# Kernel tuning notes

Hardware: AMD Instinct MI355X
Metric: run time of the kernel (lower is better)

The kernel has to match this reference:

```python
import jax, jax.numpy as jnp
import numpy as np


def _swiglu(h):
    a, b = jnp.split(h, 2, axis=-1)
    return jax.nn.silu(a) * b


def setup_inputs() -> dict:
    key = jax.random.key(0)
    ks = jax.random.split(key, 12)
    B, T, D = 4, 2048, 1024
    HD = 4096          # dense FFN hidden (swiglu -> fc1 out 2*HD)
    S, K = 1024, 4     # ssm d_state, d_conv
    E, HE = 8, 512     # n_experts, expert hidden (swiglu)
    s = 0.02
    w = lambda k_, shape: jax.random.normal(k_, shape, jnp.float32) * s
    return dict(
        x=jax.random.normal(ks[0], (B, T, D), jnp.float32),
        rW=w(ks[1], (3, D)), rb=jnp.zeros((3,), jnp.float32),
        d1W=w(ks[2], (2 * HD, D)), d1b=jnp.zeros((2 * HD,), jnp.float32),
        d2W=w(ks[3], (D, HD)), d2b=jnp.zeros((D,), jnp.float32),
        sW_in=w(ks[4], (S, D)), sb_in=jnp.zeros((S,), jnp.float32),
        sW_conv=w(ks[5], (S, S, K)), sb_conv=jnp.zeros((S,), jnp.float32),
        sW_out=w(ks[6], (D, S)), sb_out=jnp.zeros((D,), jnp.float32),
        mW=w(ks[7], (E, D)), mb=jnp.zeros((E,), jnp.float32),
        eW1=w(ks[8], (E, 2 * HE, D)), eb1=jnp.zeros((E, 2 * HE), jnp.float32),
        eW2=w(ks[9], (E, D, HE)), eb2=jnp.zeros((E, D), jnp.float32),
        k=2,
    )


def reference(x, rW, rb, d1W, d1b, d2W, d2b,
              sW_in, sb_in, sW_conv, sb_conv, sW_out, sb_out,
              mW, mb, eW1, eb1, eW2, eb2, k):
    # ---- branch router (token-level softmax, temperature=1) ----
    bw = jax.nn.softmax(x @ rW.T + rb, axis=-1)              # [B,T,3]

    # ---- branch 0: dense swiglu FFN ----
    dense = _swiglu(x @ d1W.T + d1b) @ d2W.T + d2b           # [B,T,D]

    # ---- branch 1: SSM layer (causal conv, groups=1, gate=1) ----
    h = (x @ sW_in.T + sb_in).transpose(0, 2, 1)             # [B,S,T]
    Kc = sW_conv.shape[-1]
    conv = jax.lax.conv_general_dilated(
        h, sW_conv, window_strides=(1,), padding=[(Kc - 1, 0)],
        dimension_numbers=('NCH', 'OIH', 'NCH'))
    seq = (conv + sb_conv[None, :, None]).transpose(0, 2, 1)  # [B,T,S]
    ssm = seq @ sW_out.T + sb_out                             # [B,T,D]

    # ---- branch 2: MoE (top-k softmax router, dense-dispatch reference) ----
    E = mW.shape[0]
    logits = x @ mW.T + mb                                    # [B,T,E]
    vals, idx = jax.lax.top_k(logits, k)                      # [B,T,k]
    wk = jax.nn.softmax(vals, axis=-1)
    combine = jnp.sum(jax.nn.one_hot(idx, E, dtype=x.dtype) * wk[..., None], axis=-2)  # [B,T,E]
    h1 = _swiglu(jnp.einsum('btd,efd->btef', x, eW1) + eb1)   # [B,T,E,HE]
    eout = jnp.einsum('bteh,edh->bted', h1, eW2) + eb2        # [B,T,E,D]
    moe = jnp.einsum('bted,bte->btd', eout, combine)          # [B,T,D]

    return bw[..., 0:1] * dense + bw[..., 1:2] * ssm + bw[..., 2:3] * moe
```

## Files before the change

kernel.cpp:

```cpp
#include <hip/hip_runtime.h>
#include <hip/hip_bf16.h>
#include <cstdint>

typedef __bf16 bf16_t;
typedef __bf16 bf16x8 __attribute__((ext_vector_type(8)));
typedef float f32x4 __attribute__((ext_vector_type(4)));

#define DEV_INLINE __device__ __forceinline__

#define NTOK 8192
#define DDIM 1024
#define HDIM 4096
#define SDIM 1024
#define NEXP 8
#define HEXP 512
#define TSEQ 2048
#define MAXTILES 136
#define MAXROWS (MAXTILES * 128)

#define VMCNT(n) asm volatile("s_waitcnt vmcnt(" #n ")" ::: "memory")
#define BARF() asm volatile("s_barrier" ::: "memory")

__global__ __launch_bounds__(256) void k_f32_to_bf16(const float* __restrict__ src,
                                                     bf16_t* __restrict__ dst, int n8) {
  int i = blockIdx.x * 256 + threadIdx.x;
  if (i >= n8) return;
  const float4* s = (const float4*)src + (size_t)i * 2;
  float4 v0 = s[0], v1 = s[1];
  bf16x8 o;
  o[0] = (bf16_t)v0.x; o[1] = (bf16_t)v0.y; o[2] = (bf16_t)v0.z; o[3] = (bf16_t)v0.w;
  o[4] = (bf16_t)v1.x; o[5] = (bf16_t)v1.y; o[6] = (bf16_t)v1.z; o[7] = (bf16_t)v1.w;
  *((bf16x8*)dst + i) = o;
}

__global__ __launch_bounds__(256) void k_convw(const float* __restrict__ src,
                                               bf16_t* __restrict__ dst) {
  int i = blockIdx.x * 256 + threadIdx.x;
  size_t flat = (size_t)i * 8;
  int s = (int)(flat >> 12);
  int col = (int)(flat & 4095);
  int k = col >> 10;
  int si0 = col & 1023;
  const float* sp = src + (size_t)s * 4096 + k;
  bf16x8 o;
#pragma unroll
  for (int j = 0; j < 8; ++j) o[j] = (bf16_t)sp[(size_t)(si0 + j) * 4];
  *(bf16x8*)(dst + flat) = o;
}

__global__ __launch_bounds__(256) void k_zero(int* cnt, int* fill, int* idx,
                                              bf16_t* zpad) {
  int i = blockIdx.x * 256 + threadIdx.x;
  if (i < NEXP) { cnt[i] = 0; fill[i] = 0; }
  if (i < 128) zpad[i] = (bf16_t)0.f;
  if (i < MAXROWS) idx[i] = 0;
}

__global__ __launch_bounds__(1024) void k_count(const int* __restrict__ top2e,
                                                int* __restrict__ cnt) {
  __shared__ int hist[NEXP];
  const int tid = threadIdx.x;
  if (tid < NEXP) hist[tid] = 0;
  __syncthreads();
  int c[NEXP];
#pragma unroll
  for (int e = 0; e < NEXP; ++e) c[e] = 0;
#pragma unroll
  for (int j = 0; j < 2 * NTOK / 1024; ++j) {
    int v = top2e[j * 1024 + tid];
#pragma unroll
    for (int e = 0; e < NEXP; ++e) c[e] += (v == e) ? 1 : 0;
  }
#pragma unroll
  for (int e = 0; e < NEXP; ++e)
    for (int off = 32; off; off >>= 1) c[e] += __shfl_xor(c[e], off);
  if ((tid & 63) == 0) {
#pragma unroll
    for (int e = 0; e < NEXP; ++e) atomicAdd(&hist[e], c[e]);
  }
  __syncthreads();
  if (tid < NEXP) cnt[tid] = hist[tid];
}

__global__ void k_scan(const int* __restrict__ cnt, int* __restrict__ base,
                       int* __restrict__ ntiles, int* __restrict__ tile_e,
                       int* __restrict__ tile_row) {
  if (threadIdx.x == 0 && blockIdx.x == 0) {
    int b = 0, tt = 0;
    for (int e = 0; e < NEXP; ++e) {
      base[e] = b;
      int nt = (cnt[e] + 127) >> 7;
      for (int j = 0; j < nt; ++j) { tile_e[tt] = e; tile_row[tt] = b + j * 128; ++tt; }
      b += nt * 128;
    }
    *ntiles = tt;
  }
}

__global__ __launch_bounds__(256) void k_scatter(const int* __restrict__ top2e,
                                                 const float* __restrict__ top2w,
                                                 const int* __restrict__ base,
                                                 int* __restrict__ fill,
                                                 int* __restrict__ idx,
                                                 int* __restrict__ slotmap) {
  __shared__ int lcnt[NEXP];
  __shared__ int lbase[NEXP];
  const int tid = threadIdx.x;
  const int t = blockIdx.x * 256 + tid;
  if (tid < NEXP) lcnt[tid] = 0;
  __syncthreads();
  const int e0 = top2e[t * 2 + 0], e1 = top2e[t * 2 + 1];
  const int s0 = atomicAdd(&lcnt[e0], 1);
  const int s1 = atomicAdd(&lcnt[e1], 1);
  __syncthreads();
  if (tid < NEXP) lbase[tid] = atomicAdd(&fill[tid], lcnt[tid]);
  __syncthreads();
  const int p0 = base[e0] + lbase[e0] + s0;
  const int p1 = base[e1] + lbase[e1] + s1;
  idx[p0] = t; idx[p1] = t;
  slotmap[t * 2 + 0] = p0;
  slotmap[t * 2 + 1] = p1;
}

__global__ __launch_bounds__(256) void k_router(const float* __restrict__ x,
                                                const float* __restrict__ rW,
                                                const float* __restrict__ rb,
                                                const float* __restrict__ mW,
                                                const float* __restrict__ mb,
                                                float* __restrict__ bw3,
                                                int* __restrict__ top2e,
                                                float* __restrict__ top2w) {
  int wave = threadIdx.x >> 6, lane = threadIdx.x & 63;
  int t = blockIdx.x * 4 + wave;
  const float* xr = x + (size_t)t * DDIM;
  float xv[16];
#pragma unroll
  for (int i = 0; i < 16; i += 4) *(float4*)&xv[i] = *(const float4*)&xr[lane * 16 + i];
  float acc[11];
#pragma unroll
  for (int j = 0; j < 11; ++j) {
    const float* w = (j < 3) ? (rW + j * DDIM) : (mW + (j - 3) * DDIM);
    float s = 0.f;
#pragma unroll
    for (int i = 0; i < 16; i += 4) {
      float4 wv = *(const float4*)&w[lane * 16 + i];
      s += xv[i] * wv.x + xv[i + 1] * wv.y + xv[i + 2] * wv.z + xv[i + 3] * wv.w;
    }
    acc[j] = s;
  }
#pragma unroll
  for (int j = 0; j < 11; ++j)
    for (int off = 32; off; off >>= 1) acc[j] += __shfl_xor(acc[j], off);
  if (lane == 0) {
    float l0 = acc[0] + rb[0], l1 = acc[1] + rb[1], l2 = acc[2] + rb[2];
    float mx = fmaxf(l0, fmaxf(l1, l2));
    float e0 = expf(l0 - mx), e1 = expf(l1 - mx), e2 = expf(l2 - mx);
    float inv = 1.f / (e0 + e1 + e2);
    float w2 = e2 * inv;
    bw3[t * 3 + 0] = e0 * inv; bw3[t * 3 + 1] = e1 * inv; bw3[t * 3 + 2] = w2;
    float lg[8];
#pragma unroll
    for (int e = 0; e < 8; ++e) lg[e] = acc[3 + e] + mb[e];
    int i0 = 0;
#pragma unroll
    for (int e = 1; e < 8; ++e) if (lg[e] > lg[i0]) i0 = e;
    int i1 = -1;
#pragma unroll
    for (int e = 0; e < 8; ++e) {
      if (e == i0) continue;
      if (i1 < 0 || lg[e] > lg[i1]) i1 = e;
    }
    float ee = expf(lg[i1] - lg[i0]);
    float w0 = 1.f / (1.f + ee), w1 = ee / (1.f + ee);
    top2e[t * 2 + 0] = i0; top2e[t * 2 + 1] = i1;
    top2w[t * 2 + 0] = w2 * w0; top2w[t * 2 + 1] = w2 * w1;
  }
}

__global__ __launch_bounds__(256) void k_combine(const bf16_t* __restrict__ eo,
                                                 const int* __restrict__ slotmap,
                                                 const float* __restrict__ top2w,
                                                 float* __restrict__ out) {
  int wave = threadIdx.x >> 6, lane = threadIdx.x & 63;
  int t = blockIdx.x * 4 + wave;
  const int s0 = slotmap[t * 2 + 0], s1 = slotmap[t * 2 + 1];
  const float g0 = top2w[t * 2 + 0], g1 = top2w[t * 2 + 1];
  const bf16x8* r0 = (const bf16x8*)(eo + (size_t)s0 * DDIM);
  const bf16x8* r1 = (const bf16x8*)(eo + (size_t)s1 * DDIM);
  float* orow = out + (size_t)t * DDIM;
#pragma unroll
  for (int i = 0; i < 2; ++i) {
    const int d = lane + i * 64;
    bf16x8 a = r0[d], b = r1[d];
    float vo[8];
    *(float4*)&vo[0] = *(const float4*)&orow[d * 8];
    *(float4*)&vo[4] = *(const float4*)&orow[d * 8 + 4];
#pragma unroll
    for (int j = 0; j < 8; ++j) vo[j] += g0 * (float)a[j] + g1 * (float)b[j];
    *(float4*)&orow[d * 8] = *(float4*)&vo[0];
    *(float4*)&orow[d * 8 + 4] = *(float4*)&vo[4];
  }
}

DEV_INLINE void gload16(const bf16_t* g, bf16_t* l) {
  __builtin_amdgcn_global_load_lds((const __attribute__((address_space(1))) void*)g,
                                   (__attribute__((address_space(3))) void*)l, 16, 0, 0);
}

DEV_INLINE void blockmap(int& bx, int& by) {
  const int nbx = gridDim.x, nby = gridDim.y;
  int id = blockIdx.x + nbx * blockIdx.y;
  const int nwg = nbx * nby;
  if ((nwg & 7) == 0) id = (id & 7) * (nwg >> 3) + (id >> 3);
  bx = id % nbx;
  by = id / nbx;
}

constexpr int EPI_BF16 = 0;
constexpr int EPI_OUT_W = 1;
constexpr int EPI_OUT_A = 2;

template <int EPI>
__global__ __launch_bounds__(256) void k_gemm(
    const bf16_t* __restrict__ A, const bf16_t* __restrict__ B,
    bf16_t* __restrict__ Cb, float* __restrict__ Cf,
    const float* __restrict__ bias, const float* __restrict__ scale, int sstride,
    int N, int K) {
  constexpr int BUF = 16384;
  __shared__ __align__(16) char lds[2 * BUF];

  const int tid = threadIdx.x;
  const int lane = tid & 63;
  const int wave = tid >> 6;
  const int lr = lane & 15;
  const int hi = lane >> 4;

  int bx, by;
  blockmap(bx, by);

  const int bm = by * 128;
  const int bn = bx * 128;
  const int wm = (wave >> 1) * 64;
  const int wn = (wave & 1) * 64;

  const int srow = tid >> 2;
  const int scol = 8 * ((tid & 3) ^ ((tid >> 3) & 3));
  const bf16_t* Asrc = A + (size_t)(bm + srow) * K + scol;
  const bf16_t* Bsrc = B + (size_t)(bn + srow) * K + scol;
  const size_t r64K = (size_t)64 * K;
  const int NT = K >> 5;

  f32x4 acc[4][4];
#pragma unroll
  for (int a = 0; a < 4; ++a)
#pragma unroll
    for (int b = 0; b < 4; ++b)
#pragma unroll
      for (int j = 0; j < 4; ++j) acc[a][b][j] = 0.f;

  auto stage = [&](int t) {
    char* l = lds + (t & 1) * BUF + tid * 16;
    const bf16_t* ga = Asrc + (size_t)t * 32;
    const bf16_t* gb = Bsrc + (size_t)t * 32;
    gload16(ga, (bf16_t*)l);
    gload16(ga + r64K, (bf16_t*)(l + 4096));
    gload16(gb, (bf16_t*)(l + 8192));
    gload16(gb + r64K, (bf16_t*)(l + 12288));
  };
  auto rdA = [&](int buf, int row) -> bf16x8 {
    int off = buf + (row << 6) + ((hi ^ ((row >> 1) & 3)) << 4);
    return *(const bf16x8*)(lds + off);
  };
  auto rdB = [&](int buf, int row) -> bf16x8 {
    int off = buf + 8192 + (row << 6) + ((hi ^ ((row >> 1) & 3)) << 4);
    return *(const bf16x8*)(lds + off);
  };

  stage(0);

  for (int t = 0; t < NT; ++t) {
    VMCNT(0);
    BARF();
    const int buf = (t & 1) * BUF;
    bf16x8 bfr[4], afr[4];
#pragma unroll
    for (int ni = 0; ni < 4; ++ni) bfr[ni] = rdB(buf, wn + ni * 16 + lr);
#pragma unroll
    for (int i = 0; i < 4; ++i) afr[i] = rdA(buf, wm + i * 16 + lr);
    if (t + 1 < NT) stage(t + 1);
    __builtin_amdgcn_s_setprio(1);
#pragma unroll
    for (int i = 0; i < 4; ++i)
#pragma unroll
      for (int ni = 0; ni < 4; ++ni)
        acc[i][ni] = __builtin_amdgcn_mfma_f32_16x16x32_bf16(afr[i], bfr[ni], acc[i][ni], 0, 0, 0);
    __builtin_amdgcn_s_setprio(0);
  }

  float bv[4];
#pragma unroll
  for (int ni = 0; ni < 4; ++ni) bv[ni] = bias[bn + wn + ni * 16 + lr];
#pragma unroll
  for (int mi = 0; mi < 4; ++mi) {
#pragma unroll
    for (int j = 0; j < 4; ++j) {
      const int rowg = bm + wm + mi * 16 + hi * 4 + j;
      float sc = 0.f;
      if constexpr (EPI == EPI_OUT_W || EPI == EPI_OUT_A)
        sc = scale[(size_t)rowg * sstride];
#pragma unroll
      for (int ni = 0; ni < 4; ++ni) {
        const int colg = bn + wn + ni * 16 + lr;
        float v = acc[mi][ni][j] + bv[ni];
        if constexpr (EPI == EPI_BF16) {
          Cb[(size_t)rowg * N + colg] = (bf16_t)v;
        } else if constexpr (EPI == EPI_OUT_W) {
          Cf[(size_t)rowg * N + colg] = sc * v;
        } else {
          Cf[(size_t)rowg * N + colg] += sc * v;
        }
      }
    }
  }
}

__global__ __launch_bounds__(256) void k_gemm_fc1(
    const bf16_t* __restrict__ A, const bf16_t* __restrict__ Ba,
    const bf16_t* __restrict__ Bb, bf16_t* __restrict__ C,
    const float* __restrict__ bias_a, const float* __restrict__ bias_b,
    int N, int K) {
  constexpr int BUF = 16384;
  __shared__ __align__(16) char lds[2 * BUF];

  const int tid = threadIdx.x;
  const int lane = tid & 63;
  const int wave = tid >> 6;
  const int lr = lane & 15;
  const int hi = lane >> 4;

  int bx, by;
  blockmap(bx, by);

  const int bm = by * 128;
  const int bn = bx * 64;
  const int wm = (wave >> 1) * 64;
  const int wn = (wave & 1) * 32;

  const int srow = tid >> 2;
  const int scol = 8 * ((tid & 3) ^ ((tid >> 3) & 3));
  const bf16_t* Asrc = A + (size_t)(bm + srow) * K + scol;
  const bf16_t* Basrc = Ba + (size_t)(bn + srow) * K + scol;
  const bf16_t* Bbsrc = Bb + (size_t)(bn + srow) * K + scol;
  const size_t r64K = (size_t)64 * K;
  const int NT = K >> 5;

  f32x4 aca[4][2], acb[4][2];
#pragma unroll
  for (int a = 0; a < 4; ++a)
#pragma unroll
    for (int b = 0; b < 2; ++b)
#pragma unroll
      for (int j = 0; j < 4; ++j) { aca[a][b][j] = 0.f; acb[a][b][j] = 0.f; }

  auto stage = [&](int t) {
    char* l = lds + (t & 1) * BUF + tid * 16;
    const bf16_t* ga = Asrc + (size_t)t * 32;
    gload16(ga, (bf16_t*)l);
    gload16(ga + r64K, (bf16_t*)(l + 4096));
    gload16(Basrc + (size_t)t * 32, (bf16_t*)(l + 8192));
    gload16(Bbsrc + (size_t)t * 32, (bf16_t*)(l + 12288));
  };
  auto rd = [&](int base, int row) -> bf16x8 {
    int off = base + (row << 6) + ((hi ^ ((row >> 1) & 3)) << 4);
    return *(const bf16x8*)(lds + off);
  };

  stage(0);

  for (int t = 0; t < NT; ++t) {
    VMCNT(0);
    BARF();
    const int buf = (t & 1) * BUF;
    bf16x8 afr[4], bfa[2], bfb[2];
#pragma unroll
    for (int i = 0; i < 4; ++i) afr[i] = rd(buf, wm + i * 16 + lr);
#pragma unroll
    for (int ni = 0; ni < 2; ++ni) bfa[ni] = rd(buf + 8192, wn + ni * 16 + lr);
#pragma unroll
    for (int ni = 0; ni < 2; ++ni) bfb[ni] = rd(buf + 12288, wn + ni * 16 + lr);
    if (t + 1 < NT) stage(t + 1);
    __builtin_amdgcn_s_setprio(1);
#pragma unroll
    for (int i = 0; i < 4; ++i)
#pragma unroll
      for (int ni = 0; ni < 2; ++ni) {
        aca[i][ni] = __builtin_amdgcn_mfma_f32_16x16x32_bf16(afr[i], bfa[ni], aca[i][ni], 0, 0, 0);
        acb[i][ni] = __builtin_amdgcn_mfma_f32_16x16x32_bf16(afr[i], bfb[ni], acb[i][ni], 0, 0, 0);
      }
    __builtin_amdgcn_s_setprio(0);
  }

  float bva[2], bvb[2];
#pragma unroll
  for (int ni = 0; ni < 2; ++ni) {
    bva[ni] = bias_a[bn + wn + ni * 16 + lr];
    bvb[ni] = bias_b[bn + wn + ni * 16 + lr];
  }
#pragma unroll
  for (int mi = 0; mi < 4; ++mi) {
#pragma unroll
    for (int j = 0; j < 4; ++j) {
      const int rowg = bm + wm + mi * 16 + hi * 4 + j;
#pragma unroll
      for (int ni = 0; ni < 2; ++ni) {
        const int colg = bn + wn + ni * 16 + lr;
        float va = aca[mi][ni][j] + bva[ni];
        float vb = acb[mi][ni][j] + bvb[ni];
        float s = va / (1.f + __expf(-va));
        C[(size_t)rowg * N + colg] = (bf16_t)(s * vb);
      }
    }
  }
}

__global__ __launch_bounds__(256) void k_gemm_conv(
    const bf16_t* __restrict__ h, const bf16_t* __restrict__ Bw,
    bf16_t* __restrict__ Cb, const float* __restrict__ bias,
    const bf16_t* __restrict__ zpad) {
  constexpr int N = SDIM;
  constexpr int K = SDIM * 4;
  constexpr int BUF = 16384;
  __shared__ __align__(16) char lds[2 * BUF];

  const int tid = threadIdx.x;
  const int lane = tid & 63;
  const int wave = tid >> 6;
  const int lr = lane & 15;
  const int hi = lane >> 4;

  int bx, by;
  blockmap(bx, by);

  const int bm = by * 128;
  const int bn = bx * 128;
  const int wm = (wave >> 1) * 64;
  const int wn = (wave & 1) * 64;

  const int srow = tid >> 2;
  const int scol = 8 * ((tid & 3) ^ ((tid >> 3) & 3));
  const int row0 = bm + srow;
  const int tt0 = row0 & (TSEQ - 1);
  const bf16_t* Bsrc = Bw + (size_t)(bn + srow) * K + scol;
  const size_t r64K = (size_t)64 * K;
  const int NT = K >> 5;

  f32x4 acc[4][4];
#pragma unroll
  for (int a = 0; a < 4; ++a)
#pragma unroll
    for (int b = 0; b < 4; ++b)
#pragma unroll
      for (int j = 0; j < 4; ++j) acc[a][b][j] = 0.f;

  auto stage = [&](int t) {
    char* l = lds + (t & 1) * BUF + tid * 16;
    const int k = t >> 5;
    const int si = (t & 31) * 32 + scol;
    const bf16_t* ga0 = (tt0 + k >= 3)
        ? h + (size_t)(row0 + k - 3) * SDIM + si : zpad;
    const bf16_t* ga1 = h + (size_t)(row0 + 64 + k - 3) * SDIM + si;
    gload16(ga0, (bf16_t*)l);
    gload16(ga1, (bf16_t*)(l + 4096));
    const bf16_t* gb = Bsrc + (size_t)t * 32;
    gload16(gb, (bf16_t*)(l + 8192));
    gload16(gb + r64K, (bf16_t*)(l + 12288));
  };
  auto rdA = [&](int buf, int row) -> bf16x8 {
    int off = buf + (row << 6) + ((hi ^ ((row >> 1) & 3)) << 4);
    return *(const bf16x8*)(lds + off);
  };
  auto rdB = [&](int buf, int row) -> bf16x8 {
    int off = buf + 8192 + (row << 6) + ((hi ^ ((row >> 1) & 3)) << 4);
    return *(const bf16x8*)(lds + off);
  };

  stage(0);

  for (int t = 0; t < NT; ++t) {
    VMCNT(0);
    BARF();
    const int buf = (t & 1) * BUF;
    bf16x8 bfr[4], afr[4];
#pragma unroll
    for (int ni = 0; ni < 4; ++ni) bfr[ni] = rdB(buf, wn + ni * 16 + lr);
#pragma unroll
    for (int i = 0; i < 4; ++i) afr[i] = rdA(buf, wm + i * 16 + lr);
    if (t + 1 < NT) stage(t + 1);
    __builtin_amdgcn_s_setprio(1);
#pragma unroll
    for (int i = 0; i < 4; ++i)
#pragma unroll
      for (int ni = 0; ni < 4; ++ni)
        acc[i][ni] = __builtin_amdgcn_mfma_f32_16x16x32_bf16(afr[i], bfr[ni], acc[i][ni], 0, 0, 0);
    __builtin_amdgcn_s_setprio(0);
  }

  float bv[4];
#pragma unroll
  for (int ni = 0; ni < 4; ++ni) bv[ni] = bias[bn + wn + ni * 16 + lr];
#pragma unroll
  for (int mi = 0; mi < 4; ++mi) {
#pragma unroll
    for (int j = 0; j < 4; ++j) {
      const int rowg = bm + wm + mi * 16 + hi * 4 + j;
#pragma unroll
      for (int ni = 0; ni < 4; ++ni) {
        const int colg = bn + wn + ni * 16 + lr;
        Cb[(size_t)rowg * N + colg] = (bf16_t)(acc[mi][ni][j] + bv[ni]);
      }
    }
  }
}

__global__ __launch_bounds__(256) void k_moe_fc1(
    const bf16_t* __restrict__ A, const bf16_t* __restrict__ Bw, size_t zB,
    bf16_t* __restrict__ C, const float* __restrict__ bias, int bstride,
    const int* __restrict__ ntiles_p, const int* __restrict__ tile_e,
    const int* __restrict__ tile_row, const int* __restrict__ idx,
    int N, int K) {
  constexpr int BUF = 16384;
  __shared__ __align__(16) char lds[2 * BUF];

  const int tid = threadIdx.x;
  const int lane = tid & 63;
  const int wave = tid >> 6;
  const int lr = lane & 15;
  const int hi = lane >> 4;

  const int nbx = gridDim.x, nby = gridDim.y;
  int id = blockIdx.x + nbx * blockIdx.y;
  const int nwg = nbx * nby;
  if ((nwg & 7) == 0) id = (id & 7) * (nwg >> 3) + (id >> 3);
  const int bx = id % nbx;
  const int by = id / nbx;

  const int ntiles = *ntiles_p;
  if (bx >= ntiles) return;
  const int e = tile_e[bx];
  const int bm = tile_row[bx];
  const int bn = by * 64;
  const int wm = (wave >> 1) * 64;
  const int wn = (wave & 1) * 32;

  const int srow = tid >> 2;
  const int scol = 8 * ((tid & 3) ^ ((tid >> 3) & 3));
  const int atok0 = idx[bm + srow];
  const int atok1 = idx[bm + srow + 64];
  const bf16_t* Asrc0 = A + (size_t)atok0 * K + scol;
  const bf16_t* Asrc1 = A + (size_t)atok1 * K + scol;
  const bf16_t* Basrc = Bw + (size_t)e * zB + (size_t)(bn + srow) * K + scol;
  const bf16_t* Bbsrc = Basrc + (size_t)HEXP * K;
  const int NT = K >> 5;

  f32x4 aca[4][2], acb[4][2];
#pragma unroll
  for (int a = 0; a < 4; ++a)
#pragma unroll
    for (int b = 0; b < 2; ++b)
#pragma unroll
      for (int j = 0; j < 4; ++j) { aca[a][b][j] = 0.f; acb[a][b][j] = 0.f; }

  auto stage = [&](int t) {
    char* l = lds + (t & 1) * BUF + tid * 16;
    gload16(Asrc0 + (size_t)t * 32, (bf16_t*)l);
    gload16(Asrc1 + (size_t)t * 32, (bf16_t*)(l + 4096));
    gload16(Basrc + (size_t)t * 32, (bf16_t*)(l + 8192));
    gload16(Bbsrc + (size_t)t * 32, (bf16_t*)(l + 12288));
  };
  auto rd = [&](int base, int row) -> bf16x8 {
    int off = base + (row << 6) + ((hi ^ ((row >> 1) & 3)) << 4);
    return *(const bf16x8*)(lds + off);
  };

  stage(0);

  for (int t = 0; t < NT; ++t) {
    VMCNT(0);
    BARF();
    const int buf = (t & 1) * BUF;
    bf16x8 afr[4], bfa[2], bfb[2];
#pragma unroll
    for (int i = 0; i < 4; ++i) afr[i] = rd(buf, wm + i * 16 + lr);
#pragma unroll
    for (int ni = 0; ni < 2; ++ni) bfa[ni] = rd(buf + 8192, wn + ni * 16 + lr);
#pragma unroll
    for (int ni = 0; ni < 2; ++ni) bfb[ni] = rd(buf + 12288, wn + ni * 16 + lr);
    if (t + 1 < NT) stage(t + 1);
    __builtin_amdgcn_s_setprio(1);
#pragma unroll
    for (int i = 0; i < 4; ++i)
#pragma unroll
      for (int ni = 0; ni < 2; ++ni) {
        aca[i][ni] = __builtin_amdgcn_mfma_f32_16x16x32_bf16(afr[i], bfa[ni], aca[i][ni], 0, 0, 0);
        acb[i][ni] = __builtin_amdgcn_mfma_f32_16x16x32_bf16(afr[i], bfb[ni], acb[i][ni], 0, 0, 0);
      }
    __builtin_amdgcn_s_setprio(0);
  }

  const float* bpa = bias + (size_t)e * bstride;
  const float* bpb = bpa + HEXP;
  float bva[2], bvb[2];
#pragma unroll
  for (int ni = 0; ni < 2; ++ni) {
    bva[ni] = bpa[bn + wn + ni * 16 + lr];
    bvb[ni] = bpb[bn + wn + ni * 16 + lr];
  }
#pragma unroll
  for (int mi = 0; mi < 4; ++mi) {
#pragma unroll
    for (int j = 0; j < 4; ++j) {
      const int slot = bm + wm + mi * 16 + hi * 4 + j;
#pragma unroll
      for (int ni = 0; ni < 2; ++ni) {
        const int colg = bn + wn + ni * 16 + lr;
        float va = aca[mi][ni][j] + bva[ni];
        float vb = acb[mi][ni][j] + bvb[ni];
        float s = va / (1.f + __expf(-va));
        C[(size_t)slot * N + colg] = (bf16_t)(s * vb);
      }
    }
  }
}

__global__ __launch_bounds__(256) void k_moe_fc2(
    const bf16_t* __restrict__ A, const bf16_t* __restrict__ Bw, size_t zB,
    bf16_t* __restrict__ Cb, const float* __restrict__ bias, int bstride,
    const int* __restrict__ ntiles_p, const int* __restrict__ tile_e,
    const int* __restrict__ tile_row,
    int N, int K) {
  constexpr int BUF = 16384;
  __shared__ __align__(16) char lds[2 * BUF];

  const int tid = threadIdx.x;
  const int lane = tid & 63;
  const int wave = tid >> 6;
  const int lr = lane & 15;
  const int hi = lane >> 4;

  const int nbx = gridDim.x, nby = gridDim.y;
  int id = blockIdx.x + nbx * blockIdx.y;
  const int nwg = nbx * nby;
  if ((nwg & 7) == 0) id = (id & 7) * (nwg >> 3) + (id >> 3);
  const int bx = id % nbx;
  const int by = id / nbx;

  const int ntiles = *ntiles_p;
  if (bx >= ntiles) return;
  const int e = tile_e[bx];
  const int bm = tile_row[bx];
  const int bn = by * 128;
  const int wm = (wave >> 1) * 64;
  const int wn = (wave & 1) * 64;

  const int srow = tid >> 2;
  const int scol = 8 * ((tid & 3) ^ ((tid >> 3) & 3));
  const bf16_t* Asrc = A + (size_t)(bm + srow) * K + scol;
  const bf16_t* Bsrc = Bw + (size_t)e * zB + (size_t)(bn + srow) * K + scol;
  const size_t r64K = (size_t)64 * K;
  const int NT = K >> 5;

  f32x4 acc[4][4];
#pragma unroll
  for (int a = 0; a < 4; ++a)
#pragma unroll
    for (int b = 0; b < 4; ++b)
#pragma unroll
      for (int j = 0; j < 4; ++j) acc[a][b][j] = 0.f;

  auto stage = [&](int t) {
    char* l = lds + (t & 1) * BUF + tid * 16;
    gload16(Asrc + (size_t)t * 32, (bf16_t*)l);
    gload16(Asrc + (size_t)t * 32 + r64K, (bf16_t*)(l + 4096));
    gload16(Bsrc + (size_t)t * 32, (bf16_t*)(l + 8192));
    gload16(Bsrc + (size_t)t * 32 + r64K, (bf16_t*)(l + 12288));
  };
  auto rdA = [&](int buf, int row) -> bf16x8 {
    int off = buf + (row << 6) + ((hi ^ ((row >> 1) & 3)) << 4);
    return *(const bf16x8*)(lds + off);
  };
  auto rdB = [&](int buf, int row) -> bf16x8 {
    int off = buf + 8192 + (row << 6) + ((hi ^ ((row >> 1) & 3)) << 4);
    return *(const bf16x8*)(lds + off);
  };

  stage(0);

  for (int t = 0; t < NT; ++t) {
    VMCNT(0);
    BARF();
    const int buf = (t & 1) * BUF;
    bf16x8 bfr[4], afr[4];
#pragma unroll
    for (int ni = 0; ni < 4; ++ni) bfr[ni] = rdB(buf, wn + ni * 16 + lr);
#pragma unroll
    for (int i = 0; i < 4; ++i) afr[i] = rdA(buf, wm + i * 16 + lr);
    if (t + 1 < NT) stage(t + 1);
    __builtin_amdgcn_s_setprio(1);
#pragma unroll
    for (int i = 0; i < 4; ++i)
#pragma unroll
      for (int ni = 0; ni < 4; ++ni)
        acc[i][ni] = __builtin_amdgcn_mfma_f32_16x16x32_bf16(afr[i], bfr[ni], acc[i][ni], 0, 0, 0);
    __builtin_amdgcn_s_setprio(0);
  }

  const float* bp = bias + (size_t)e * bstride;
  float bv[4];
#pragma unroll
  for (int ni = 0; ni < 4; ++ni) bv[ni] = bp[bn + wn + ni * 16 + lr];
#pragma unroll
  for (int mi = 0; mi < 4; ++mi) {
#pragma unroll
    for (int j = 0; j < 4; ++j) {
      const int slot = bm + wm + mi * 16 + hi * 4 + j;
#pragma unroll
      for (int ni = 0; ni < 4; ++ni) {
        const int colg = bn + wn + ni * 16 + lr;
        Cb[(size_t)slot * N + colg] = (bf16_t)(acc[mi][ni][j] + bv[ni]);
      }
    }
  }
}

extern "C" void kernel_launch(void* const* d_in, const int* in_sizes, int n_in,
                              void* d_out, int out_size, void* d_ws, size_t ws_size,
                              hipStream_t stream) {
  (void)in_sizes; (void)n_in; (void)out_size; (void)ws_size;
  const float* x    = (const float*)d_in[0];
  const float* rW   = (const float*)d_in[1];
  const float* rb   = (const float*)d_in[2];
  const float* d1W  = (const float*)d_in[3];
  const float* d1b  = (const float*)d_in[4];
  const float* d2W  = (const float*)d_in[5];
  const float* d2b  = (const float*)d_in[6];
  const float* sWin = (const float*)d_in[7];
  const float* sbin = (const float*)d_in[8];
  const float* sWc  = (const float*)d_in[9];
  const float* sbc  = (const float*)d_in[10];
  const float* sWo  = (const float*)d_in[11];
  const float* sbo  = (const float*)d_in[12];
  const float* mW   = (const float*)d_in[13];
  const float* mb   = (const float*)d_in[14];
  const float* eW1  = (const float*)d_in[15];
  const float* eb1  = (const float*)d_in[16];
  const float* eW2  = (const float*)d_in[17];
  const float* eb2  = (const float*)d_in[18];
  float* out = (float*)d_out;

  char* ws = (char*)d_ws;
  size_t off = 0;
  auto alloc = [&](size_t bytes) -> void* {
    void* p = ws + off;
    off += (bytes + 255) & ~(size_t)255;
    return p;
  };
  bf16_t* xb    = (bf16_t*)alloc((size_t)NTOK * DDIM * 2);
  bf16_t* wd1   = (bf16_t*)alloc((size_t)2 * HDIM * DDIM * 2);
  bf16_t* wd2   = (bf16_t*)alloc((size_t)DDIM * HDIM * 2);
  bf16_t* wsin  = (bf16_t*)alloc((size_t)SDIM * DDIM * 2);
  bf16_t* wconv = (bf16_t*)alloc((size_t)SDIM * SDIM * 4 * 2);
  bf16_t* wsout = (bf16_t*)alloc((size_t)DDIM * SDIM * 2);
  bf16_t* we1   = (bf16_t*)alloc((size_t)NEXP * 2 * HEXP * DDIM * 2);
  bf16_t* we2   = (bf16_t*)alloc((size_t)NEXP * DDIM * HEXP * 2);
  bf16_t* Cc    = (bf16_t*)alloc((size_t)NTOK * HDIM * 2);
  bf16_t* Dd    = (bf16_t*)alloc((size_t)NTOK * HDIM * 2);
  bf16_t* th    = (bf16_t*)alloc((size_t)NTOK * SDIM * 2);
  bf16_t* tsq   = (bf16_t*)alloc((size_t)NTOK * SDIM * 2);
  float*  bw3   = (float*)alloc((size_t)NTOK * 3 * 4);
  int*    top2e = (int*)alloc((size_t)NTOK * 2 * 4);
  float*  top2w = (float*)alloc((size_t)NTOK * 2 * 4);
  int*    slotm = (int*)alloc((size_t)NTOK * 2 * 4);
  int*    cnt   = (int*)alloc(NEXP * 4);
  int*    fill  = (int*)alloc(NEXP * 4);
  int*    basep = (int*)alloc((NEXP + 1) * 4);
  int*    ntl   = (int*)alloc(4);
  int*    t_e   = (int*)alloc(MAXTILES * 4);
  int*    t_row = (int*)alloc(MAXTILES * 4);
  int*    idx   = (int*)alloc(MAXROWS * 4);
  bf16_t* zpad  = (bf16_t*)alloc(256);
  bf16_t* eo    = Dd;

  k_f32_to_bf16<<<4096, 256, 0, stream>>>(x, xb, NTOK * DDIM / 8);
  k_f32_to_bf16<<<4096, 256, 0, stream>>>(d1W, wd1, 2 * HDIM * DDIM / 8);
  k_f32_to_bf16<<<2048, 256, 0, stream>>>(d2W, wd2, DDIM * HDIM / 8);
  k_f32_to_bf16<<<512, 256, 0, stream>>>(sWin, wsin, SDIM * DDIM / 8);
  k_convw<<<2048, 256, 0, stream>>>(sWc, wconv);
  k_f32_to_bf16<<<512, 256, 0, stream>>>(sWo, wsout, DDIM * SDIM / 8);
  k_f32_to_bf16<<<4096, 256, 0, stream>>>(eW1, we1, NEXP * 2 * HEXP * DDIM / 8);
  k_f32_to_bf16<<<2048, 256, 0, stream>>>(eW2, we2, NEXP * DDIM * HEXP / 8);
  k_zero<<<(MAXROWS + 255) / 256, 256, 0, stream>>>(cnt, fill, idx, zpad);
  k_router<<<2048, 256, 0, stream>>>(x, rW, rb, mW, mb, bw3, top2e, top2w);
  k_count<<<1, 1024, 0, stream>>>(top2e, cnt);
  k_scan<<<1, 64, 0, stream>>>(cnt, basep, ntl, t_e, t_row);
  k_scatter<<<NTOK / 256, 256, 0, stream>>>(top2e, top2w, basep, fill, idx, slotm);

  k_gemm_fc1<<<dim3(64, 64), 256, 0, stream>>>(
      xb, wd1, wd1 + (size_t)HDIM * DDIM, Cc, d1b, d1b + HDIM, HDIM, DDIM);
  k_gemm<EPI_OUT_W><<<dim3(8, 64), 256, 0, stream>>>(
      Cc, wd2, nullptr, out, d2b, bw3, 3, DDIM, HDIM);

  k_moe_fc1<<<dim3(MAXTILES, 8), 256, 0, stream>>>(
      xb, we1, (size_t)2 * HEXP * DDIM, Cc, eb1, 2 * HEXP,
      ntl, t_e, t_row, idx, HEXP, DDIM);
  k_moe_fc2<<<dim3(MAXTILES, 8), 256, 0, stream>>>(
      Cc, we2, (size_t)DDIM * HEXP, eo, eb2, DDIM,
      ntl, t_e, t_row, DDIM, HEXP);
  k_combine<<<NTOK / 4, 256, 0, stream>>>(eo, slotm, top2w, out);

  k_gemm<EPI_BF16><<<dim3(8, 64), 256, 0, stream>>>(
      xb, wsin, th, nullptr, sbin, nullptr, 0, SDIM, DDIM);
  k_gemm_conv<<<dim3(8, 64), 256, 0, stream>>>(th, wconv, tsq, sbc, zpad);
  k_gemm<EPI_OUT_A><<<dim3(8, 64), 256, 0, stream>>>(
      tsq, wsout, nullptr, out, sbo, bw3 + 1, 3, DDIM, SDIM);
}
```

Baseline: 594.1 us.

## Merge independent GEMMs into phase mega-kernels and fuse setup conversions

Turns each GEMM body into a device function and dispatches several of them from combined launches by block-id range. Dense fc1, MoE fc1 and SSM in-projection share phase1, while dense fc2, the conv GEMM and MoE fc2 share phase2. The weight conversions, router and zeroing become one setup kernel, and count and scan merge into one. The aim is fewer launches and filling the GPU with independent work instead of running small-grid GEMMs back to back. The cost is more complex block-id dispatch and a separate MoE intermediate buffer carved from Dd.

```diff
diff --git a/kernel.cpp b/kernel.cpp
--- a/kernel.cpp
+++ b/kernel.cpp
@@ -21,10 +21,520 @@
 #define VMCNT(n) asm volatile("s_waitcnt vmcnt(" #n ")" ::: "memory")
 #define BARF() asm volatile("s_barrier" ::: "memory")
 
-__global__ __launch_bounds__(256) void k_f32_to_bf16(const float* __restrict__ src,
-                                                     bf16_t* __restrict__ dst, int n8) {
-  int i = blockIdx.x * 256 + threadIdx.x;
-  if (i >= n8) return;
+DEV_INLINE void gload16(const bf16_t* g, bf16_t* l) {
+  __builtin_amdgcn_global_load_lds((const __attribute__((address_space(1))) void*)g,
+                                   (__attribute__((address_space(3))) void*)l, 16, 0, 0);
+}
+
+DEV_INLINE void submap(int sub, int nbx, int nby, int& bx, int& by) {
+  const int nwg = nbx * nby;
+  int id = sub;
+  if ((nwg & 7) == 0) id = (id & 7) * (nwg >> 3) + (id >> 3);
+  bx = id % nbx;
+  by = id / nbx;
+}
+
+constexpr int EPI_BF16 = 0;
+constexpr int EPI_OUT_W = 1;
+constexpr int EPI_OUT_A = 2;
+
+template <int EPI>
+DEV_INLINE void dev_gemm(char* lds, int sub, int nbx, int nby,
+                         const bf16_t* __restrict__ A, const bf16_t* __restrict__ B,
+                         bf16_t* __restrict__ Cb, float* __restrict__ Cf,
+                         const float* __restrict__ bias,
+                         const float* __restrict__ scale, int sstride,
+                         int N, int K) {
+  constexpr int BUF = 16384;
+  const int tid = threadIdx.x;
+  const int lane = tid & 63;
+  const int wave = tid >> 6;
+  const int lr = lane & 15;
+  const int hi = lane >> 4;
+
+  int bx, by;
+  submap(sub, nbx, nby, bx, by);
+
+  const int bm = by * 128;
+  const int bn = bx * 128;
+  const int wm = (wave >> 1) * 64;
+  const int wn = (wave & 1) * 64;
+
+  const int srow = tid >> 2;
+  const int scol = 8 * ((tid & 3) ^ ((tid >> 3) & 3));
+  const bf16_t* Asrc = A + (size_t)(bm + srow) * K + scol;
+  const bf16_t* Bsrc = B + (size_t)(bn + srow) * K + scol;
+  const size_t r64K = (size_t)64 * K;
+  const int NT = K >> 5;
+
+  f32x4 acc[4][4];
+#pragma unroll
+  for (int a = 0; a < 4; ++a)
+#pragma unroll
+    for (int b = 0; b < 4; ++b)
+#pragma unroll
+      for (int j = 0; j < 4; ++j) acc[a][b][j] = 0.f;
+
+  auto stage = [&](int t) {
+    char* l = lds + (t & 1) * BUF + tid * 16;
+    const bf16_t* ga = Asrc + (size_t)t * 32;
+    const bf16_t* gb = Bsrc + (size_t)t * 32;
+    gload16(ga, (bf16_t*)l);
+    gload16(ga + r64K, (bf16_t*)(l + 4096));
+    gload16(gb, (bf16_t*)(l + 8192));
+    gload16(gb + r64K, (bf16_t*)(l + 12288));
+  };
+  auto rdA = [&](int buf, int row) -> bf16x8 {
+    int off = buf + (row << 6) + ((hi ^ ((row >> 1) & 3)) << 4);
+    return *(const bf16x8*)(lds + off);
+  };
+  auto rdB = [&](int buf, int row) -> bf16x8 {
+    int off = buf + 8192 + (row << 6) + ((hi ^ ((row >> 1) & 3)) << 4);
+    return *(const bf16x8*)(lds + off);
+  };
+
+  stage(0);
+
+  for (int t = 0; t < NT; ++t) {
+    VMCNT(0);
+    BARF();
+    const int buf = (t & 1) * BUF;
+    bf16x8 bfr[4], afr[4];
+#pragma unroll
+    for (int ni = 0; ni < 4; ++ni) bfr[ni] = rdB(buf, wn + ni * 16 + lr);
+#pragma unroll
+    for (int i = 0; i < 4; ++i) afr[i] = rdA(buf, wm + i * 16 + lr);
+    if (t + 1 < NT) stage(t + 1);
+    __builtin_amdgcn_s_setprio(1);
+#pragma unroll
+    for (int i = 0; i < 4; ++i)
+#pragma unroll
+      for (int ni = 0; ni < 4; ++ni)
+        acc[i][ni] = __builtin_amdgcn_mfma_f32_16x16x32_bf16(afr[i], bfr[ni], acc[i][ni], 0, 0, 0);
+    __builtin_amdgcn_s_setprio(0);
+  }
+
+  float bv[4];
+#pragma unroll
+  for (int ni = 0; ni < 4; ++ni) bv[ni] = bias[bn + wn + ni * 16 + lr];
+#pragma unroll
+  for (int mi = 0; mi < 4; ++mi) {
+#pragma unroll
+    for (int j = 0; j < 4; ++j) {
+      const int rowg = bm + wm + mi * 16 + hi * 4 + j;
+      float sc = 0.f;
+      if constexpr (EPI == EPI_OUT_W || EPI == EPI_OUT_A)
+        sc = scale[(size_t)rowg * sstride];
+#pragma unroll
+      for (int ni = 0; ni < 4; ++ni) {
+        const int colg = bn + wn + ni * 16 + lr;
+        float v = acc[mi][ni][j] + bv[ni];
+        if constexpr (EPI == EPI_BF16) {
+          Cb[(size_t)rowg * N + colg] = (bf16_t)v;
+        } else if constexpr (EPI == EPI_OUT_W) {
+          Cf[(size_t)rowg * N + colg] = sc * v;
+        } else {
+          Cf[(size_t)rowg * N + colg] += sc * v;
+        }
+      }
+    }
+  }
+}
+
+DEV_INLINE void dev_gemm_fc1(char* lds, int sub,
+                             const bf16_t* __restrict__ A, const bf16_t* __restrict__ Ba,
+                             const bf16_t* __restrict__ Bb, bf16_t* __restrict__ C,
+                             const float* __restrict__ bias_a, const float* __restrict__ bias_b,
+                             int N, int K) {
+  constexpr int BUF = 16384;
+  const int tid = threadIdx.x;
+  const int lane = tid & 63;
+  const int wave = tid >> 6;
+  const int lr = lane & 15;
+  const int hi = lane >> 4;
+
+  int bx, by;
+  submap(sub, 64, 64, bx, by);
+
+  const int bm = by * 128;
+  const int bn = bx * 64;
+  const int wm = (wave >> 1) * 64;
+  const int wn = (wave & 1) * 32;
+
+  const int srow = tid >> 2;
+  const int scol = 8 * ((tid & 3) ^ ((tid >> 3) & 3));
+  const bf16_t* Asrc = A + (size_t)(bm + srow) * K + scol;
+  const bf16_t* Basrc = Ba + (size_t)(bn + srow) * K + scol;
+  const bf16_t* Bbsrc = Bb + (size_t)(bn + srow) * K + scol;
+  const size_t r64K = (size_t)64 * K;
+  const int NT = K >> 5;
+
+  f32x4 aca[4][2], acb[4][2];
+#pragma unroll
+  for (int a = 0; a < 4; ++a)
+#pragma unroll
+    for (int b = 0; b < 2; ++b)
+#pragma unroll
+      for (int j = 0; j < 4; ++j) { aca[a][b][j] = 0.f; acb[a][b][j] = 0.f; }
+
+  auto stage = [&](int t) {
+    char* l = lds + (t & 1) * BUF + tid * 16;
+    const bf16_t* ga = Asrc + (size_t)t * 32;
+    gload16(ga, (bf16_t*)l);
+    gload16(ga + r64K, (bf16_t*)(l + 4096));
+    gload16(Basrc + (size_t)t * 32, (bf16_t*)(l + 8192));
+    gload16(Bbsrc + (size_t)t * 32, (bf16_t*)(l + 12288));
+  };
+  auto rd = [&](int base, int row) -> bf16x8 {
+    int off = base + (row << 6) + ((hi ^ ((row >> 1) & 3)) << 4);
+    return *(const bf16x8*)(lds + off);
+  };
+
+  stage(0);
+
+  for (int t = 0; t < NT; ++t) {
+    VMCNT(0);
+    BARF();
+    const int buf = (t & 1) * BUF;
+    bf16x8 afr[4], bfa[2], bfb[2];
+#pragma unroll
+    for (int i = 0; i < 4; ++i) afr[i] = rd(buf, wm + i * 16 + lr);
+#pragma unroll
+    for (int ni = 0; ni < 2; ++ni) bfa[ni] = rd(buf + 8192, wn + ni * 16 + lr);
+#pragma unroll
+    for (int ni = 0; ni < 2; ++ni) bfb[ni] = rd(buf + 12288, wn + ni * 16 + lr);
+    if (t + 1 < NT) stage(t + 1);
+    __builtin_amdgcn_s_setprio(1);
+#pragma unroll
+    for (int i = 0; i < 4; ++i)
+#pragma unroll
+      for (int ni = 0; ni < 2; ++ni) {
+        aca[i][ni] = __builtin_amdgcn_mfma_f32_16x16x32_bf16(afr[i], bfa[ni], aca[i][ni], 0, 0, 0);
+        acb[i][ni] = __builtin_amdgcn_mfma_f32_16x16x32_bf16(afr[i], bfb[ni], acb[i][ni], 0, 0, 0);
+      }
+    __builtin_amdgcn_s_setprio(0);
+  }
+
+  float bva[2], bvb[2];
+#pragma unroll
+  for (int ni = 0; ni < 2; ++ni) {
+    bva[ni] = bias_a[bn + wn + ni * 16 + lr];
+    bvb[ni] = bias_b[bn + wn + ni * 16 + lr];
+  }
+#pragma unroll
+  for (int mi = 0; mi < 4; ++mi) {
+#pragma unroll
+    for (int j = 0; j < 4; ++j) {
+      const int rowg = bm + wm + mi * 16 + hi * 4 + j;
+#pragma unroll
+      for (int ni = 0; ni < 2; ++ni) {
+        const int colg = bn + wn + ni * 16 + lr;
+        float va = aca[mi][ni][j] + bva[ni];
+        float vb = acb[mi][ni][j] + bvb[ni];
+        float s = va / (1.f + __expf(-va));
+        C[(size_t)rowg * N + colg] = (bf16_t)(s * vb);
+      }
+    }
+  }
+}
+
+DEV_INLINE void dev_gemm_conv(char* lds, int sub,
+                              const bf16_t* __restrict__ h, const bf16_t* __restrict__ Bw,
+                              bf16_t* __restrict__ Cb, const float* __restrict__ bias,
+                              const bf16_t* __restrict__ zpad) {
+  constexpr int N = SDIM;
+  constexpr int K = SDIM * 4;
+  constexpr int BUF = 16384;
+  const int tid = threadIdx.x;
+  const int lane = tid & 63;
+  const int wave = tid >> 6;
+  const int lr = lane & 15;
+  const int hi = lane >> 4;
+
+  int bx, by;
+  submap(sub, 8, 64, bx, by);
+
+  const int bm = by * 128;
+  const int bn = bx * 128;
+  const int wm = (wave >> 1) * 64;
+  const int wn = (wave & 1) * 64;
+
+  const int srow = tid >> 2;
+  const int scol = 8 * ((tid & 3) ^ ((tid >> 3) & 3));
+  const int row0 = bm + srow;
+  const int tt0 = row0 & (TSEQ - 1);
+  const bf16_t* Bsrc = Bw + (size_t)(bn + srow) * K + scol;
+  const size_t r64K = (size_t)64 * K;
+  const int NT = K >> 5;
+
+  f32x4 acc[4][4];
+#pragma unroll
+  for (int a = 0; a < 4; ++a)
+#pragma unroll
+    for (int b = 0; b < 4; ++b)
+#pragma unroll
+      for (int j = 0; j < 4; ++j) acc[a][b][j] = 0.f;
+
+  auto stage = [&](int t) {
+    char* l = lds + (t & 1) * BUF + tid * 16;
+    const int k = t >> 5;
+    const int si = (t & 31) * 32 + scol;
+    const bf16_t* ga0 = (tt0 + k >= 3)
+        ? h + (size_t)(row0 + k - 3) * SDIM + si : zpad;
+    const bf16_t* ga1 = h + (size_t)(row0 + 64 + k - 3) * SDIM + si;
+    gload16(ga0, (bf16_t*)l);
+    gload16(ga1, (bf16_t*)(l + 4096));
+    const bf16_t* gb = Bsrc + (size_t)t * 32;
+    gload16(gb, (bf16_t*)(l + 8192));
+    gload16(gb + r64K, (bf16_t*)(l + 12288));
+  };
+  auto rdA = [&](int buf, int row) -> bf16x8 {
+    int off = buf + (row << 6) + ((hi ^ ((row >> 1) & 3)) << 4);
+    return *(const bf16x8*)(lds + off);
+  };
+  auto rdB = [&](int buf, int row) -> bf16x8 {
+    int off = buf + 8192 + (row << 6) + ((hi ^ ((row >> 1) & 3)) << 4);
+    return *(const bf16x8*)(lds + off);
+  };
+
+  stage(0);
+
+  for (int t = 0; t < NT; ++t) {
+    VMCNT(0);
+    BARF();
+    const int buf = (t & 1) * BUF;
+    bf16x8 bfr[4], afr[4];
+#pragma unroll
+    for (int ni = 0; ni < 4; ++ni) bfr[ni] = rdB(buf, wn + ni * 16 + lr);
+#pragma unroll
+    for (int i = 0; i < 4; ++i) afr[i] = rdA(buf, wm + i * 16 + lr);
+    if (t + 1 < NT) stage(t + 1);
+    __builtin_amdgcn_s_setprio(1);
+#pragma unroll
+    for (int i = 0; i < 4; ++i)
+#pragma unroll
+      for (int ni = 0; ni < 4; ++ni)
+        acc[i][ni] = __builtin_amdgcn_mfma_f32_16x16x32_bf16(afr[i], bfr[ni], acc[i][ni], 0, 0, 0);
+    __builtin_amdgcn_s_setprio(0);
+  }
+
+  float bv[4];
+#pragma unroll
+  for (int ni = 0; ni < 4; ++ni) bv[ni] = bias[bn + wn + ni * 16 + lr];
+#pragma unroll
+  for (int mi = 0; mi < 4; ++mi) {
+#pragma unroll
+    for (int j = 0; j < 4; ++j) {
+      const int rowg = bm + wm + mi * 16 + hi * 4 + j;
+#pragma unroll
+      for (int ni = 0; ni < 4; ++ni) {
+        const int colg = bn + wn + ni * 16 + lr;
+        Cb[(size_t)rowg * N + colg] = (bf16_t)(acc[mi][ni][j] + bv[ni]);
+      }
+    }
+  }
+}
+
+DEV_INLINE void dev_moe_fc1(char* lds, int sub,
+                            const bf16_t* __restrict__ A, const bf16_t* __restrict__ Bw, size_t zB,
+                            bf16_t* __restrict__ C, const float* __restrict__ bias, int bstride,
+                            const int* __restrict__ ntiles_p, const int* __restrict__ tile_e,
+                            const int* __restrict__ tile_row, const int* __restrict__ idx,
+                            int N, int K) {
+  constexpr int BUF = 16384;
+  const int tid = threadIdx.x;
+  const int lane = tid & 63;
+  const int wave = tid >> 6;
+  const int lr = lane & 15;
+  const int hi = lane >> 4;
+
+  int bx, by;
+  submap(sub, MAXTILES, 8, bx, by);
+
+  const int ntiles = *ntiles_p;
+  if (bx >= ntiles) return;
+  const int e = tile_e[bx];
+  const int bm = tile_row[bx];
+  const int bn = by * 64;
+  const int wm = (wave >> 1) * 64;
+  const int wn = (wave & 1) * 32;
+
+  const int srow = tid >> 2;
+  const int scol = 8 * ((tid & 3) ^ ((tid >> 3) & 3));
+  const int atok0 = idx[bm + srow];
+  const int atok1 = idx[bm + srow + 64];
+  const bf16_t* Asrc0 = A + (size_t)atok0 * K + scol;
+  const bf16_t* Asrc1 = A + (size_t)atok1 * K + scol;
+  const bf16_t* Basrc = Bw + (size_t)e * zB + (size_t)(bn + srow) * K + scol;
+  const bf16_t* Bbsrc = Basrc + (size_t)HEXP * K;
+  const int NT = K >> 5;
+
+  f32x4 aca[4][2], acb[4][2];
+#pragma unroll
+  for (int a = 0; a < 4; ++a)
+#pragma unroll
+    for (int b = 0; b < 2; ++b)
+#pragma unroll
+      for (int j = 0; j < 4; ++j) { aca[a][b][j] = 0.f; acb[a][b][j] = 0.f; }
+
+  auto stage = [&](int t) {
+    char* l = lds + (t & 1) * BUF + tid * 16;
+    gload16(Asrc0 + (size_t)t * 32, (bf16_t*)l);
+    gload16(Asrc1 + (size_t)t * 32, (bf16_t*)(l + 4096));
+    gload16(Basrc + (size_t)t * 32, (bf16_t*)(l + 8192));
+    gload16(Bbsrc + (size_t)t * 32, (bf16_t*)(l + 12288));
+  };
+  auto rd = [&](int base, int row) -> bf16x8 {
+    int off = base + (row << 6) + ((hi ^ ((row >> 1) & 3)) << 4);
+    return *(const bf16x8*)(lds + off);
+  };
+
+  stage(0);
+
+  for (int t = 0; t < NT; ++t) {
+    VMCNT(0);
+    BARF();
+    const int buf = (t & 1) * BUF;
+    bf16x8 afr[4], bfa[2], bfb[2];
+#pragma unroll
+    for (int i = 0; i < 4; ++i) afr[i] = rd(buf, wm + i * 16 + lr);
+#pragma unroll
+    for (int ni = 0; ni < 2; ++ni) bfa[ni] = rd(buf + 8192, wn + ni * 16 + lr);
+#pragma unroll
+    for (int ni = 0; ni < 2; ++ni) bfb[ni] = rd(buf + 12288, wn + ni * 16 + lr);
+    if (t + 1 < NT) stage(t + 1);
+    __builtin_amdgcn_s_setprio(1);
+#pragma unroll
+    for (int i = 0; i < 4; ++i)
+#pragma unroll
+      for (int ni = 0; ni < 2; ++ni) {
+        aca[i][ni] = __builtin_amdgcn_mfma_f32_16x16x32_bf16(afr[i], bfa[ni], aca[i][ni], 0, 0, 0);
+        acb[i][ni] = __builtin_amdgcn_mfma_f32_16x16x32_bf16(afr[i], bfb[ni], acb[i][ni], 0, 0, 0);
+      }
+    __builtin_amdgcn_s_setprio(0);
+  }
+
+  const float* bpa = bias + (size_t)e * bstride;
+  const float* bpb = bpa + HEXP;
+  float bva[2], bvb[2];
+#pragma unroll
+  for (int ni = 0; ni < 2; ++ni) {
+    bva[ni] = bpa[bn + wn + ni * 16 + lr];
+    bvb[ni] = bpb[bn + wn + ni * 16 + lr];
+  }
+#pragma unroll
+  for (int mi = 0; mi < 4; ++mi) {
+#pragma unroll
+    for (int j = 0; j < 4; ++j) {
+      const int slot = bm + wm + mi * 16 + hi * 4 + j;
+#pragma unroll
+      for (int ni = 0; ni < 2; ++ni) {
+        const int colg = bn + wn + ni * 16 + lr;
+        float va = aca[mi][ni][j] + bva[ni];
+        float vb = acb[mi][ni][j] + bvb[ni];
+        float s = va / (1.f + __expf(-va));
+        C[(size_t)slot * N + colg] = (bf16_t)(s * vb);
+      }
+    }
+  }
+}
+
+DEV_INLINE void dev_moe_fc2(char* lds, int sub,
+                            const bf16_t* __restrict__ A, const bf16_t* __restrict__ Bw, size_t zB,
+                            bf16_t* __restrict__ Cb, const float* __restrict__ bias, int bstride,
+                            const int* __restrict__ ntiles_p, const int* __restrict__ tile_e,
+                            const int* __restrict__ tile_row,
+                            int N, int K) {
+  constexpr int BUF = 16384;
+  const int tid = threadIdx.x;
+  const int lane = tid & 63;
+  const int wave = tid >> 6;
+  const int lr = lane & 15;
+  const int hi = lane >> 4;
+
+  int bx, by;
+  submap(sub, MAXTILES, 8, bx, by);
+
+  const int ntiles = *ntiles_p;
+  if (bx >= ntiles) return;
+  const int e = tile_e[bx];
+  const int bm = tile_row[bx];
+  const int bn = by * 128;
+  const int wm = (wave >> 1) * 64;
+  const int wn = (wave & 1) * 64;
+
+  const int srow = tid >> 2;
+  const int scol = 8 * ((tid & 3) ^ ((tid >> 3) & 3));
+  const bf16_t* Asrc = A + (size_t)(bm + srow) * K + scol;
+  const bf16_t* Bsrc = Bw + (size_t)e * zB + (size_t)(bn + srow) * K + scol;
+  const size_t r64K = (size_t)64 * K;
+  const int NT = K >> 5;
+
+  f32x4 acc[4][4];
+#pragma unroll
+  for (int a = 0; a < 4; ++a)
+#pragma unroll
+    for (int b = 0; b < 4; ++b)
+#pragma unroll
+      for (int j = 0; j < 4; ++j) acc[a][b][j] = 0.f;
+
+  auto stage = [&](int t) {
+    char* l = lds + (t & 1) * BUF + tid * 16;
+    gload16(Asrc + (size_t)t * 32, (bf16_t*)l);
+    gload16(Asrc + (size_t)t * 32 + r64K, (bf16_t*)(l + 4096));
+    gload16(Bsrc + (size_t)t * 32, (bf16_t*)(l + 8192));
+    gload16(Bsrc + (size_t)t * 32 + r64K, (bf16_t*)(l + 12288));
+  };
+  auto rdA = [&](int buf, int row) -> bf16x8 {
+    int off = buf + (row << 6) + ((hi ^ ((row >> 1) & 3)) << 4);
+    return *(const bf16x8*)(lds + off);
+  };
+  auto rdB = [&](int buf, int row) -> bf16x8 {
+    int off = buf + 8192 + (row << 6) + ((hi ^ ((row >> 1) & 3)) << 4);
+    return *(const bf16x8*)(lds + off);
+  };
+
+  stage(0);
+
+  for (int t = 0; t < NT; ++t) {
+    VMCNT(0);
+    BARF();
+    const int buf = (t & 1) * BUF;
+    bf16x8 bfr[4], afr[4];
+#pragma unroll
+    for (int ni = 0; ni < 4; ++ni) bfr[ni] = rdB(buf, wn + ni * 16 + lr);
+#pragma unroll
+    for (int i = 0; i < 4; ++i) afr[i] = rdA(buf, wm + i * 16 + lr);
+    if (t + 1 < NT) stage(t + 1);
+    __builtin_amdgcn_s_setprio(1);
+#pragma unroll
+    for (int i = 0; i < 4; ++i)
+#pragma unroll
+      for (int ni = 0; ni < 4; ++ni)
+        acc[i][ni] = __builtin_amdgcn_mfma_f32_16x16x32_bf16(afr[i], bfr[ni], acc[i][ni], 0, 0, 0);
+    __builtin_amdgcn_s_setprio(0);
+  }
+
+  const float* bp = bias + (size_t)e * bstride;
+  float bv[4];
+#pragma unroll
+  for (int ni = 0; ni < 4; ++ni) bv[ni] = bp[bn + wn + ni * 16 + lr];
+#pragma unroll
+  for (int mi = 0; mi < 4; ++mi) {
+#pragma unroll
+    for (int j = 0; j < 4; ++j) {
+      const int slot = bm + wm + mi * 16 + hi * 4 + j;
+#pragma unroll
+      for (int ni = 0; ni < 4; ++ni) {
+        const int colg = bn + wn + ni * 16 + lr;
+        Cb[(size_t)slot * N + colg] = (bf16_t)(acc[mi][ni][j] + bv[ni]);
+      }
+    }
+  }
+}
+
+DEV_INLINE void dev_conv8(const float* __restrict__ src, bf16_t* __restrict__ dst, int sub) {
+  int i = sub * 256 + threadIdx.x;
   const float4* s = (const float4*)src + (size_t)i * 2;
   float4 v0 = s[0], v1 = s[1];
   bf16x8 o;
@@ -33,31 +543,99 @@
   *((bf16x8*)dst + i) = o;
 }
 
-__global__ __launch_bounds__(256) void k_convw(const float* __restrict__ src,
-                                               bf16_t* __restrict__ dst) {
-  int i = blockIdx.x * 256 + threadIdx.x;
-  size_t flat = (size_t)i * 8;
-  int s = (int)(flat >> 12);
-  int col = (int)(flat & 4095);
-  int k = col >> 10;
-  int si0 = col & 1023;
-  const float* sp = src + (size_t)s * 4096 + k;
-  bf16x8 o;
-#pragma unroll
-  for (int j = 0; j < 8; ++j) o[j] = (bf16_t)sp[(size_t)(si0 + j) * 4];
-  *(bf16x8*)(dst + flat) = o;
-}
-
-__global__ __launch_bounds__(256) void k_zero(int* cnt, int* fill, int* idx,
-                                              bf16_t* zpad) {
-  int i = blockIdx.x * 256 + threadIdx.x;
-  if (i < NEXP) { cnt[i] = 0; fill[i] = 0; }
+__global__ __launch_bounds__(256) void k_setup(
+    const float* __restrict__ x, const float* __restrict__ d1W,
+    const float* __restrict__ d2W, const float* __restrict__ sWin,
+    const float* __restrict__ sWo, const float* __restrict__ eW1,
+    const float* __restrict__ eW2, const float* __restrict__ sWc,
+    const float* __restrict__ rW, const float* __restrict__ rb,
+    const float* __restrict__ mW, const float* __restrict__ mb,
+    bf16_t* __restrict__ xb, bf16_t* __restrict__ wd1, bf16_t* __restrict__ wd2,
+    bf16_t* __restrict__ wsin, bf16_t* __restrict__ wsout,
+    bf16_t* __restrict__ we1, bf16_t* __restrict__ we2, bf16_t* __restrict__ wconv,
+    float* __restrict__ bw3, int* __restrict__ top2e, float* __restrict__ top2w,
+    int* __restrict__ fill, int* __restrict__ idx, bf16_t* __restrict__ zpad) {
+  const int b = blockIdx.x;
+  if (b < 4096) { dev_conv8(x, xb, b); return; }
+  if (b < 8192) { dev_conv8(d1W, wd1, b - 4096); return; }
+  if (b < 10240) { dev_conv8(d2W, wd2, b - 8192); return; }
+  if (b < 10752) { dev_conv8(sWin, wsin, b - 10240); return; }
+  if (b < 11264) { dev_conv8(sWo, wsout, b - 10752); return; }
+  if (b < 15360) { dev_conv8(eW1, we1, b - 11264); return; }
+  if (b < 17408) { dev_conv8(eW2, we2, b - 15360); return; }
+  if (b < 19456) {
+    int i = (b - 17408) * 256 + threadIdx.x;
+    size_t flat = (size_t)i * 8;
+    int s = (int)(flat >> 12);
+    int col = (int)(flat & 4095);
+    int k = col >> 10;
+    int si0 = col & 1023;
+    const float* sp = sWc + (size_t)s * 4096 + k;
+    bf16x8 o;
+#pragma unroll
+    for (int j = 0; j < 8; ++j) o[j] = (bf16_t)sp[(size_t)(si0 + j) * 4];
+    *(bf16x8*)(wconv + flat) = o;
+    return;
+  }
+  if (b < 21504) {
+    int wave = threadIdx.x >> 6, lane = threadIdx.x & 63;
+    int t = (b - 19456) * 4 + wave;
+    const float* xr = x + (size_t)t * DDIM;
+    float xv[16];
+#pragma unroll
+    for (int i = 0; i < 16; i += 4) *(float4*)&xv[i] = *(const float4*)&xr[lane * 16 + i];
+    float acc[11];
+#pragma unroll
+    for (int j = 0; j < 11; ++j) {
+      const float* w = (j < 3) ? (rW + j * DDIM) : (mW + (j - 3) * DDIM);
+      float s = 0.f;
+#pragma unroll
+      for (int i = 0; i < 16; i += 4) {
+        float4 wv = *(const float4*)&w[lane * 16 + i];
+        s += xv[i] * wv.x + xv[i + 1] * wv.y + xv[i + 2] * wv.z + xv[i + 3] * wv.w;
+      }
+      acc[j] = s;
+    }
+#pragma unroll
+    for (int j = 0; j < 11; ++j)
+      for (int off = 32; off; off >>= 1) acc[j] += __shfl_xor(acc[j], off);
+    if (lane == 0) {
+      float l0 = acc[0] + rb[0], l1 = acc[1] + rb[1], l2 = acc[2] + rb[2];
+      float mx = fmaxf(l0, fmaxf(l1, l2));
+      float e0 = expf(l0 - mx), e1 = expf(l1 - mx), e2 = expf(l2 - mx);
+      float inv = 1.f / (e0 + e1 + e2);
+      float w2 = e2 * inv;
+      bw3[t * 3 + 0] = e0 * inv; bw3[t * 3 + 1] = e1 * inv; bw3[t * 3 + 2] = w2;
+      float lg[8];
+#pragma unroll
+      for (int e = 0; e < 8; ++e) lg[e] = acc[3 + e] + mb[e];
+      int i0 = 0;
+#pragma unroll
+      for (int e = 1; e < 8; ++e) if (lg[e] > lg[i0]) i0 = e;
+      int i1 = -1;
+#pragma unroll
+      for (int e = 0; e < 8; ++e) {
+        if (e == i0) continue;
+        if (i1 < 0 || lg[e] > lg[i1]) i1 = e;
+      }
+      float ee = expf(lg[i1] - lg[i0]);
+      float w0 = 1.f / (1.f + ee), w1 = ee / (1.f + ee);
+      top2e[t * 2 + 0] = i0; top2e[t * 2 + 1] = i1;
+      top2w[t * 2 + 0] = w2 * w0; top2w[t * 2 + 1] = w2 * w1;
+    }
+    return;
+  }
+  int i = (b - 21504) * 256 + threadIdx.x;
+  if (i < NEXP) fill[i] = 0;
   if (i < 128) zpad[i] = (bf16_t)0.f;
   if (i < MAXROWS) idx[i] = 0;
 }
 
-__global__ __launch_bounds__(1024) void k_count(const int* __restrict__ top2e,
-                                                int* __restrict__ cnt) {
+__global__ __launch_bounds__(1024) void k_count_scan(const int* __restrict__ top2e,
+                                                     int* __restrict__ base,
+                                                     int* __restrict__ ntiles,
+                                                     int* __restrict__ tile_e,
+                                                     int* __restrict__ tile_row) {
   __shared__ int hist[NEXP];
   const int tid = threadIdx.x;
   if (tid < NEXP) hist[tid] = 0;
@@ -79,17 +657,11 @@
     for (int e = 0; e < NEXP; ++e) atomicAdd(&hist[e], c[e]);
   }
   __syncthreads();
-  if (tid < NEXP) cnt[tid] = hist[tid];
-}
-
-__global__ void k_scan(const int* __restrict__ cnt, int* __restrict__ base,
-                       int* __restrict__ ntiles, int* __restrict__ tile_e,
-                       int* __restrict__ tile_row) {
-  if (threadIdx.x == 0 && blockIdx.x == 0) {
+  if (tid == 0) {
     int b = 0, tt = 0;
     for (int e = 0; e < NEXP; ++e) {
       base[e] = b;
-      int nt = (cnt[e] + 127) >> 7;
+      int nt = (hist[e] + 127) >> 7;
       for (int j = 0; j < nt; ++j) { tile_e[tt] = e; tile_row[tt] = b + j * 128; ++tt; }
       b += nt * 128;
     }
@@ -122,59 +694,60 @@
   slotmap[t * 2 + 1] = p1;
 }
 
-__global__ __launch_bounds__(256) void k_router(const float* __restrict__ x,
-                                                const float* __restrict__ rW,
-                                                const float* __restrict__ rb,
-                                                const float* __restrict__ mW,
-                                                const float* __restrict__ mb,
-                                                float* __restrict__ bw3,
-                                                int* __restrict__ top2e,
-                                                float* __restrict__ top2w) {
-  int wave = threadIdx.x >> 6, lane = threadIdx.x & 63;
-  int t = blockIdx.x * 4 + wave;
-  const float* xr = x + (size_t)t * DDIM;
-  float xv[16];
-#pragma unroll
-  for (int i = 0; i < 16; i += 4) *(float4*)&xv[i] = *(const float4*)&xr[lane * 16 + i];
-  float acc[11];
-#pragma unroll
-  for (int j = 0; j < 11; ++j) {
-    const float* w = (j < 3) ? (rW + j * DDIM) : (mW + (j - 3) * DDIM);
-    float s = 0.f;
-#pragma unroll
-    for (int i = 0; i < 16; i += 4) {
-      float4 wv = *(const float4*)&w[lane * 16 + i];
-      s += xv[i] * wv.x + xv[i + 1] * wv.y + xv[i + 2] * wv.z + xv[i + 3] * wv.w;
-    }
-    acc[j] = s;
-  }
-#pragma unroll
-  for (int j = 0; j < 11; ++j)
-    for (int off = 32; off; off >>= 1) acc[j] += __shfl_xor(acc[j], off);
-  if (lane == 0) {
-    float l0 = acc[0] + rb[0], l1 = acc[1] + rb[1], l2 = acc[2] + rb[2];
-    float mx = fmaxf(l0, fmaxf(l1, l2));
-    float e0 = expf(l0 - mx), e1 = expf(l1 - mx), e2 = expf(l2 - mx);
-    float inv = 1.f / (e0 + e1 + e2);
-    float w2 = e2 * inv;
-    bw3[t * 3 + 0] = e0 * inv; bw3[t * 3 + 1] = e1 * inv; bw3[t * 3 + 2] = w2;
-    float lg[8];
-#pragma unroll
-    for (int e = 0; e < 8; ++e) lg[e] = acc[3 + e] + mb[e];
-    int i0 = 0;
-#pragma unroll
-    for (int e = 1; e < 8; ++e) if (lg[e] > lg[i0]) i0 = e;
-    int i1 = -1;
-#pragma unroll
-    for (int e = 0; e < 8; ++e) {
-      if (e == i0) continue;
-      if (i1 < 0 || lg[e] > lg[i1]) i1 = e;
-    }
-    float ee = expf(lg[i1] - lg[i0]);
-    float w0 = 1.f / (1.f + ee), w1 = ee / (1.f + ee);
-    top2e[t * 2 + 0] = i0; top2e[t * 2 + 1] = i1;
-    top2w[t * 2 + 0] = w2 * w0; top2w[t * 2 + 1] = w2 * w1;
-  }
+__global__ __launch_bounds__(256) void k_phase1(
+    const bf16_t* __restrict__ xb, const bf16_t* __restrict__ wd1,
+    const float* __restrict__ d1b, bf16_t* __restrict__ Cc,
+    const bf16_t* __restrict__ we1, const float* __restrict__ eb1,
+    bf16_t* __restrict__ mo,
+    const int* __restrict__ ntl, const int* __restrict__ t_e,
+    const int* __restrict__ t_row, const int* __restrict__ idx,
+    const bf16_t* __restrict__ wsin, const float* __restrict__ sbin,
+    bf16_t* __restrict__ th) {
+  __shared__ __align__(16) char lds[32768];
+  const int b = blockIdx.x;
+  if (b < 4096) {
+    dev_gemm_fc1(lds, b, xb, wd1, wd1 + (size_t)HDIM * DDIM, Cc, d1b, d1b + HDIM,
+                 HDIM, DDIM);
+  } else if (b < 5184) {
+    dev_moe_fc1(lds, b - 4096, xb, we1, (size_t)2 * HEXP * DDIM, mo, eb1, 2 * HEXP,
+                ntl, t_e, t_row, idx, HEXP, DDIM);
+  } else {
+    dev_gemm<EPI_BF16>(lds, b - 5184, 8, 64, xb, wsin, th, nullptr, sbin,
+                       nullptr, 0, SDIM, DDIM);
+  }
+}
+
+__global__ __launch_bounds__(256) void k_phase2(
+    const bf16_t* __restrict__ Cc, const bf16_t* __restrict__ wd2,
+    const float* __restrict__ d2b, const float* __restrict__ bw3,
+    float* __restrict__ out,
+    const bf16_t* __restrict__ th, const bf16_t* __restrict__ wconv,
+    const float* __restrict__ sbc, bf16_t* __restrict__ tsq,
+    const bf16_t* __restrict__ zpad,
+    const bf16_t* __restrict__ mo, const bf16_t* __restrict__ we2,
+    const float* __restrict__ eb2, bf16_t* __restrict__ eo,
+    const int* __restrict__ ntl, const int* __restrict__ t_e,
+    const int* __restrict__ t_row) {
+  __shared__ __align__(16) char lds[32768];
+  const int b = blockIdx.x;
+  if (b < 512) {
+    dev_gemm<EPI_OUT_W>(lds, b, 8, 64, Cc, wd2, nullptr, out, d2b, bw3, 3,
+                        DDIM, HDIM);
+  } else if (b < 1024) {
+    dev_gemm_conv(lds, b - 512, th, wconv, tsq, sbc, zpad);
+  } else {
+    dev_moe_fc2(lds, b - 1024, mo, we2, (size_t)DDIM * HEXP, eo, eb2, DDIM,
+                ntl, t_e, t_row, DDIM, HEXP);
+  }
+}
+
+__global__ __launch_bounds__(256) void k_wsout(
+    const bf16_t* __restrict__ tsq, const bf16_t* __restrict__ wsout,
+    float* __restrict__ out, const float* __restrict__ sbo,
+    const float* __restrict__ bw3) {
+  __shared__ __align__(16) char lds[32768];
+  dev_gemm<EPI_OUT_A>(lds, blockIdx.x, 8, 64, tsq, wsout, nullptr, out, sbo,
+                      bw3 + 1, 3, DDIM, SDIM);
 }
 
 __global__ __launch_bounds__(256) void k_combine(const bf16_t* __restrict__ eo,
@@ -199,536 +772,6 @@
     for (int j = 0; j < 8; ++j) vo[j] += g0 * (float)a[j] + g1 * (float)b[j];
     *(float4*)&orow[d * 8] = *(float4*)&vo[0];
     *(float4*)&orow[d * 8 + 4] = *(float4*)&vo[4];
-  }
-}
-
-DEV_INLINE void gload16(const bf16_t* g, bf16_t* l) {
-  __builtin_amdgcn_global_load_lds((const __attribute__((address_space(1))) void*)g,
-                                   (__attribute__((address_space(3))) void*)l, 16, 0, 0);
-}
-
-DEV_INLINE void blockmap(int& bx, int& by) {
-  const int nbx = gridDim.x, nby = gridDim.y;
-  int id = blockIdx.x + nbx * blockIdx.y;
-  const int nwg = nbx * nby;
-  if ((nwg & 7) == 0) id = (id & 7) * (nwg >> 3) + (id >> 3);
-  bx = id % nbx;
-  by = id / nbx;
-}
-
-constexpr int EPI_BF16 = 0;
-constexpr int EPI_OUT_W = 1;
-constexpr int EPI_OUT_A = 2;
-
-template <int EPI>
-__global__ __launch_bounds__(256) void k_gemm(
-    const bf16_t* __restrict__ A, const bf16_t* __restrict__ B,
-    bf16_t* __restrict__ Cb, float* __restrict__ Cf,
-    const float* __restrict__ bias, const float* __restrict__ scale, int sstride,
-    int N, int K) {
-  constexpr int BUF = 16384;
-  __shared__ __align__(16) char lds[2 * BUF];
-
-  const int tid = threadIdx.x;
-  const int lane = tid & 63;
-  const int wave = tid >> 6;
-  const int lr = lane & 15;
-  const int hi = lane >> 4;
-
-  int bx, by;
-  blockmap(bx, by);
-
-  const int bm = by * 128;
-  const int bn = bx * 128;
-  const int wm = (wave >> 1) * 64;
-  const int wn = (wave & 1) * 64;
-
-  const int srow = tid >> 2;
-  const int scol = 8 * ((tid & 3) ^ ((tid >> 3) & 3));
-  const bf16_t* Asrc = A + (size_t)(bm + srow) * K + scol;
-  const bf16_t* Bsrc = B + (size_t)(bn + srow) * K + scol;
-  const size_t r64K = (size_t)64 * K;
-  const int NT = K >> 5;
-
-  f32x4 acc[4][4];
-#pragma unroll
-  for (int a = 0; a < 4; ++a)
-#pragma unroll
-    for (int b = 0; b < 4; ++b)
-#pragma unroll
-      for (int j = 0; j < 4; ++j) acc[a][b][j] = 0.f;
-
-  auto stage = [&](int t) {
-    char* l = lds + (t & 1) * BUF + tid * 16;
-    const bf16_t* ga = Asrc + (size_t)t * 32;
-    const bf16_t* gb = Bsrc + (size_t)t * 32;
-    gload16(ga, (bf16_t*)l);
-    gload16(ga + r64K, (bf16_t*)(l + 4096));
-    gload16(gb, (bf16_t*)(l + 8192));
-    gload16(gb + r64K, (bf16_t*)(l + 12288));
-  };
-  auto rdA = [&](int buf, int row) -> bf16x8 {
-    int off = buf + (row << 6) + ((hi ^ ((row >> 1) & 3)) << 4);
-    return *(const bf16x8*)(lds + off);
-  };
-  auto rdB = [&](int buf, int row) -> bf16x8 {
-    int off = buf + 8192 + (row << 6) + ((hi ^ ((row >> 1) & 3)) << 4);
-    return *(const bf16x8*)(lds + off);
-  };
-
-  stage(0);
-
-  for (int t = 0; t < NT; ++t) {
-    VMCNT(0);
-    BARF();
-    const int buf = (t & 1) * BUF;
-    bf16x8 bfr[4], afr[4];
-#pragma unroll
-    for (int ni = 0; ni < 4; ++ni) bfr[ni] = rdB(buf, wn + ni * 16 + lr);
-#pragma unroll
-    for (int i = 0; i < 4; ++i) afr[i] = rdA(buf, wm + i * 16 + lr);
-    if (t + 1 < NT) stage(t + 1);
-    __builtin_amdgcn_s_setprio(1);
-#pragma unroll
-    for (int i = 0; i < 4; ++i)
-#pragma unroll
-      for (int ni = 0; ni < 4; ++ni)
-        acc[i][ni] = __builtin_amdgcn_mfma_f32_16x16x32_bf16(afr[i], bfr[ni], acc[i][ni], 0, 0, 0);
-    __builtin_amdgcn_s_setprio(0);
-  }
-
-  float bv[4];
-#pragma unroll
-  for (int ni = 0; ni < 4; ++ni) bv[ni] = bias[bn + wn + ni * 16 + lr];
-#pragma unroll
-  for (int mi = 0; mi < 4; ++mi) {
-#pragma unroll
-    for (int j = 0; j < 4; ++j) {
-      const int rowg = bm + wm + mi * 16 + hi * 4 + j;
-      float sc = 0.f;
-      if constexpr (EPI == EPI_OUT_W || EPI == EPI_OUT_A)
-        sc = scale[(size_t)rowg * sstride];
-#pragma unroll
-      for (int ni = 0; ni < 4; ++ni) {
-        const int colg = bn + wn + ni * 16 + lr;
-        float v = acc[mi][ni][j] + bv[ni];
-        if constexpr (EPI == EPI_BF16) {
-          Cb[(size_t)rowg * N + colg] = (bf16_t)v;
-        } else if constexpr (EPI == EPI_OUT_W) {
-          Cf[(size_t)rowg * N + colg] = sc * v;
-        } else {
-          Cf[(size_t)rowg * N + colg] += sc * v;
-        }
-      }
-    }
-  }
-}
-
-__global__ __launch_bounds__(256) void k_gemm_fc1(
-    const bf16_t* __restrict__ A, const bf16_t* __restrict__ Ba,
-    const bf16_t* __restrict__ Bb, bf16_t* __restrict__ C,
-    const float* __restrict__ bias_a, const float* __restrict__ bias_b,
-    int N, int K) {
-  constexpr int BUF = 16384;
-  __shared__ __align__(16) char lds[2 * BUF];
-
-  const int tid = threadIdx.x;
-  const int lane = tid & 63;
-  const int wave = tid >> 6;
-  const int lr = lane & 15;
-  const int hi = lane >> 4;
-
-  int bx, by;
-  blockmap(bx, by);
-
-  const int bm = by * 128;
-  const int bn = bx * 64;
-  const int wm = (wave >> 1) * 64;
-  const int wn = (wave & 1) * 32;
-
-  const int srow = tid >> 2;
-  const int scol = 8 * ((tid & 3) ^ ((tid >> 3) & 3));
-  const bf16_t* Asrc = A + (size_t)(bm + srow) * K + scol;
-  const bf16_t* Basrc = Ba + (size_t)(bn + srow) * K + scol;
-  const bf16_t* Bbsrc = Bb + (size_t)(bn + srow) * K + scol;
-  const size_t r64K = (size_t)64 * K;
-  const int NT = K >> 5;
-
-  f32x4 aca[4][2], acb[4][2];
-#pragma unroll
-  for (int a = 0; a < 4; ++a)
-#pragma unroll
-    for (int b = 0; b < 2; ++b)
-#pragma unroll
-      for (int j = 0; j < 4; ++j) { aca[a][b][j] = 0.f; acb[a][b][j] = 0.f; }
-
-  auto stage = [&](int t) {
-    char* l = lds + (t & 1) * BUF + tid * 16;
-    const bf16_t* ga = Asrc + (size_t)t * 32;
-    gload16(ga, (bf16_t*)l);
-    gload16(ga + r64K, (bf16_t*)(l + 4096));
-    gload16(Basrc + (size_t)t * 32, (bf16_t*)(l + 8192));
-    gload16(Bbsrc + (size_t)t * 32, (bf16_t*)(l + 12288));
-  };
-  auto rd = [&](int base, int row) -> bf16x8 {
-    int off = base + (row << 6) + ((hi ^ ((row >> 1) & 3)) << 4);
-    return *(const bf16x8*)(lds + off);
-  };
-
-  stage(0);
-
-  for (int t = 0; t < NT; ++t) {
-    VMCNT(0);
-    BARF();
-    const int buf = (t & 1) * BUF;
-    bf16x8 afr[4], bfa[2], bfb[2];
-#pragma unroll
-    for (int i = 0; i < 4; ++i) afr[i] = rd(buf, wm + i * 16 + lr);
-#pragma unroll
-    for (int ni = 0; ni < 2; ++ni) bfa[ni] = rd(buf + 8192, wn + ni * 16 + lr);
-#pragma unroll
-    for (int ni = 0; ni < 2; ++ni) bfb[ni] = rd(buf + 12288, wn + ni * 16 + lr);
-    if (t + 1 < NT) stage(t + 1);
-    __builtin_amdgcn_s_setprio(1);
-#pragma unroll
-    for (int i = 0; i < 4; ++i)
-#pragma unroll
-      for (int ni = 0; ni < 2; ++ni) {
-        aca[i][ni] = __builtin_amdgcn_mfma_f32_16x16x32_bf16(afr[i], bfa[ni], aca[i][ni], 0, 0, 0);
-        acb[i][ni] = __builtin_amdgcn_mfma_f32_16x16x32_bf16(afr[i], bfb[ni], acb[i][ni], 0, 0, 0);
-      }
-    __builtin_amdgcn_s_setprio(0);
-  }
-
-  float bva[2], bvb[2];
-#pragma unroll
-  for (int ni = 0; ni < 2; ++ni) {
-    bva[ni] = bias_a[bn + wn + ni * 16 + lr];
-    bvb[ni] = bias_b[bn + wn + ni * 16 + lr];
-  }
-#pragma unroll
-  for (int mi = 0; mi < 4; ++mi) {
-#pragma unroll
-    for (int j = 0; j < 4; ++j) {
-      const int rowg = bm + wm + mi * 16 + hi * 4 + j;
-#pragma unroll
-      for (int ni = 0; ni < 2; ++ni) {
-        const int colg = bn + wn + ni * 16 + lr;
-        float va = aca[mi][ni][j] + bva[ni];
-        float vb = acb[mi][ni][j] + bvb[ni];
-        float s = va / (1.f + __expf(-va));
-        C[(size_t)rowg * N + colg] = (bf16_t)(s * vb);
-      }
-    }
-  }
-}
-
-__global__ __launch_bounds__(256) void k_gemm_conv(
-    const bf16_t* __restrict__ h, const bf16_t* __restrict__ Bw,
-    bf16_t* __restrict__ Cb, const float* __restrict__ bias,
-    const bf16_t* __restrict__ zpad) {
-  constexpr int N = SDIM;
-  constexpr int K = SDIM * 4;
-  constexpr int BUF = 16384;
-  __shared__ __align__(16) char lds[2 * BUF];
-
-  const int tid = threadIdx.x;
-  const int lane = tid & 63;
-  const int wave = tid >> 6;
-  const int lr = lane & 15;
-  const int hi = lane >> 4;
-
-  int bx, by;
-  blockmap(bx, by);
-
-  const int bm = by * 128;
-  const int bn = bx * 128;
-  const int wm = (wave >> 1) * 64;
-  const int wn = (wave & 1) * 64;
-
-  const int srow = tid >> 2;
-  const int scol = 8 * ((tid & 3) ^ ((tid >> 3) & 3));
-  const int row0 = bm + srow;
-  const int tt0 = row0 & (TSEQ - 1);
-  const bf16_t* Bsrc = Bw + (size_t)(bn + srow) * K + scol;
-  const size_t r64K = (size_t)64 * K;
-  const int NT = K >> 5;
-
-  f32x4 acc[4][4];
-#pragma unroll
-  for (int a = 0; a < 4; ++a)
-#pragma unroll
-    for (int b = 0; b < 4; ++b)
-#pragma unroll
-      for (int j = 0; j < 4; ++j) acc[a][b][j] = 0.f;
-
-  auto stage = [&](int t) {
-    char* l = lds + (t & 1) * BUF + tid * 16;
-    const int k = t >> 5;
-    const int si = (t & 31) * 32 + scol;
-    const bf16_t* ga0 = (tt0 + k >= 3)
-        ? h + (size_t)(row0 + k - 3) * SDIM + si : zpad;
-    const bf16_t* ga1 = h + (size_t)(row0 + 64 + k - 3) * SDIM + si;
-    gload16(ga0, (bf16_t*)l);
-    gload16(ga1, (bf16_t*)(l + 4096));
-    const bf16_t* gb = Bsrc + (size_t)t * 32;
-    gload16(gb, (bf16_t*)(l + 8192));
-    gload16(gb + r64K, (bf16_t*)(l + 12288));
-  };
-  auto rdA = [&](int buf, int row) -> bf16x8 {
-    int off = buf + (row << 6) + ((hi ^ ((row >> 1) & 3)) << 4);
-    return *(const bf16x8*)(lds + off);
-  };
-  auto rdB = [&](int buf, int row) -> bf16x8 {
-    int off = buf + 8192 + (row << 6) + ((hi ^ ((row >> 1) & 3)) << 4);
-    return *(const bf16x8*)(lds + off);
-  };
-
-  stage(0);
-
-  for (int t = 0; t < NT; ++t) {
-    VMCNT(0);
-    BARF();
-    const int buf = (t & 1) * BUF;
-    bf16x8 bfr[4], afr[4];
-#pragma unroll
-    for (int ni = 0; ni < 4; ++ni) bfr[ni] = rdB(buf, wn + ni * 16 + lr);
-#pragma unroll
-    for (int i = 0; i < 4; ++i) afr[i] = rdA(buf, wm + i * 16 + lr);
-    if (t + 1 < NT) stage(t + 1);
-    __builtin_amdgcn_s_setprio(1);
-#pragma unroll
-    for (int i = 0; i < 4; ++i)
-#pragma unroll
-      for (int ni = 0; ni < 4; ++ni)
-        acc[i][ni] = __builtin_amdgcn_mfma_f32_16x16x32_bf16(afr[i], bfr[ni], acc[i][ni], 0, 0, 0);
-    __builtin_amdgcn_s_setprio(0);
-  }
-
-  float bv[4];
-#pragma unroll
-  for (int ni = 0; ni < 4; ++ni) bv[ni] = bias[bn + wn + ni * 16 + lr];
-#pragma unroll
-  for (int mi = 0; mi < 4; ++mi) {
-#pragma unroll
-    for (int j = 0; j < 4; ++j) {
-      const int rowg = bm + wm + mi * 16 + hi * 4 + j;
-#pragma unroll
-      for (int ni = 0; ni < 4; ++ni) {
-        const int colg = bn + wn + ni * 16 + lr;
-        Cb[(size_t)rowg * N + colg] = (bf16_t)(acc[mi][ni][j] + bv[ni]);
-      }
-    }
-  }
-}
-
-__global__ __launch_bounds__(256) void k_moe_fc1(
-    const bf16_t* __restrict__ A, const bf16_t* __restrict__ Bw, size_t zB,
-    bf16_t* __restrict__ C, const float* __restrict__ bias, int bstride,
-    const int* __restrict__ ntiles_p, const int* __restrict__ tile_e,
-    const int* __restrict__ tile_row, const int* __restrict__ idx,
-    int N, int K) {
-  constexpr int BUF = 16384;
-  __shared__ __align__(16) char lds[2 * BUF];
-
-  const int tid = threadIdx.x;
-  const int lane = tid & 63;
-  const int wave = tid >> 6;
-  const int lr = lane & 15;
-  const int hi = lane >> 4;
-
-  const int nbx = gridDim.x, nby = gridDim.y;
-  int id = blockIdx.x + nbx * blockIdx.y;
-  const int nwg = nbx * nby;
-  if ((nwg & 7) == 0) id = (id & 7) * (nwg >> 3) + (id >> 3);
-  const int bx = id % nbx;
-  const int by = id / nbx;
-
-  const int ntiles = *ntiles_p;
-  if (bx >= ntiles) return;
-  const int e = tile_e[bx];
-  const int bm = tile_row[bx];
-  const int bn = by * 64;
-  const int wm = (wave >> 1) * 64;
-  const int wn = (wave & 1) * 32;
-
-  const int srow = tid >> 2;
-  const int scol = 8 * ((tid & 3) ^ ((tid >> 3) & 3));
-  const int atok0 = idx[bm + srow];
-  const int atok1 = idx[bm + srow + 64];
-  const bf16_t* Asrc0 = A + (size_t)atok0 * K + scol;
-  const bf16_t* Asrc1 = A + (size_t)atok1 * K + scol;
-  const bf16_t* Basrc = Bw + (size_t)e * zB + (size_t)(bn + srow) * K + scol;
-  const bf16_t* Bbsrc = Basrc + (size_t)HEXP * K;
-  const int NT = K >> 5;
-
-  f32x4 aca[4][2], acb[4][2];
-#pragma unroll
-  for (int a = 0; a < 4; ++a)
-#pragma unroll
-    for (int b = 0; b < 2; ++b)
-#pragma unroll
-      for (int j = 0; j < 4; ++j) { aca[a][b][j] = 0.f; acb[a][b][j] = 0.f; }
-
-  auto stage = [&](int t) {
-    char* l = lds + (t & 1) * BUF + tid * 16;
-    gload16(Asrc0 + (size_t)t * 32, (bf16_t*)l);
-    gload16(Asrc1 + (size_t)t * 32, (bf16_t*)(l + 4096));
-    gload16(Basrc + (size_t)t * 32, (bf16_t*)(l + 8192));
-    gload16(Bbsrc + (size_t)t * 32, (bf16_t*)(l + 12288));
-  };
-  auto rd = [&](int base, int row) -> bf16x8 {
-    int off = base + (row << 6) + ((hi ^ ((row >> 1) & 3)) << 4);
-    return *(const bf16x8*)(lds + off);
-  };
-
-  stage(0);
-
-  for (int t = 0; t < NT; ++t) {
-    VMCNT(0);
-    BARF();
-    const int buf = (t & 1) * BUF;
-    bf16x8 afr[4], bfa[2], bfb[2];
-#pragma unroll
-    for (int i = 0; i < 4; ++i) afr[i] = rd(buf, wm + i * 16 + lr);
-#pragma unroll
-    for (int ni = 0; ni < 2; ++ni) bfa[ni] = rd(buf + 8192, wn + ni * 16 + lr);
-#pragma unroll
-    for (int ni = 0; ni < 2; ++ni) bfb[ni] = rd(buf + 12288, wn + ni * 16 + lr);
-    if (t + 1 < NT) stage(t + 1);
-    __builtin_amdgcn_s_setprio(1);
-#pragma unroll
-    for (int i = 0; i < 4; ++i)
-#pragma unroll
-      for (int ni = 0; ni < 2; ++ni) {
-        aca[i][ni] = __builtin_amdgcn_mfma_f32_16x16x32_bf16(afr[i], bfa[ni], aca[i][ni], 0, 0, 0);
-        acb[i][ni] = __builtin_amdgcn_mfma_f32_16x16x32_bf16(afr[i], bfb[ni], acb[i][ni], 0, 0, 0);
-      }
-    __builtin_amdgcn_s_setprio(0);
-  }
-
-  const float* bpa = bias + (size_t)e * bstride;
-  const float* bpb = bpa + HEXP;
-  float bva[2], bvb[2];
-#pragma unroll
-  for (int ni = 0; ni < 2; ++ni) {
-    bva[ni] = bpa[bn + wn + ni * 16 + lr];
-    bvb[ni] = bpb[bn + wn + ni * 16 + lr];
-  }
-#pragma unroll
-  for (int mi = 0; mi < 4; ++mi) {
-#pragma unroll
-    for (int j = 0; j < 4; ++j) {
-      const int slot = bm + wm + mi * 16 + hi * 4 + j;
-#pragma unroll
-      for (int ni = 0; ni < 2; ++ni) {
-        const int colg = bn + wn + ni * 16 + lr;
-        float va = aca[mi][ni][j] + bva[ni];
-        float vb = acb[mi][ni][j] + bvb[ni];
-        float s = va / (1.f + __expf(-va));
-        C[(size_t)slot * N + colg] = (bf16_t)(s * vb);
-      }
-    }
-  }
-}
-
-__global__ __launch_bounds__(256) void k_moe_fc2(
-    const bf16_t* __restrict__ A, const bf16_t* __restrict__ Bw, size_t zB,
-    bf16_t* __restrict__ Cb, const float* __restrict__ bias, int bstride,
-    const int* __restrict__ ntiles_p, const int* __restrict__ tile_e,
-    const int* __restrict__ tile_row,
-    int N, int K) {
-  constexpr int BUF = 16384;
-  __shared__ __align__(16) char lds[2 * BUF];
-
-  const int tid = threadIdx.x;
-  const int lane = tid & 63;
-  const int wave = tid >> 6;
-  const int lr = lane & 15;
-  const int hi = lane >> 4;
-
-  const int nbx = gridDim.x, nby = gridDim.y;
-  int id = blockIdx.x + nbx * blockIdx.y;
-  const int nwg = nbx * nby;
-  if ((nwg & 7) == 0) id = (id & 7) * (nwg >> 3) + (id >> 3);
-  const int bx = id % nbx;
-  const int by = id / nbx;
-
-  const int ntiles = *ntiles_p;
-  if (bx >= ntiles) return;
-  const int e = tile_e[bx];
-  const int bm = tile_row[bx];
-  const int bn = by * 128;
-  const int wm = (wave >> 1) * 64;
-  const int wn = (wave & 1) * 64;
-
-  const int srow = tid >> 2;
-  const int scol = 8 * ((tid & 3) ^ ((tid >> 3) & 3));
-  const bf16_t* Asrc = A + (size_t)(bm + srow) * K + scol;
-  const bf16_t* Bsrc = Bw + (size_t)e * zB + (size_t)(bn + srow) * K + scol;
-  const size_t r64K = (size_t)64 * K;
-  const int NT = K >> 5;
-
-  f32x4 acc[4][4];
-#pragma unroll
-  for (int a = 0; a < 4; ++a)
-#pragma unroll
-    for (int b = 0; b < 4; ++b)
-#pragma unroll
-      for (int j = 0; j < 4; ++j) acc[a][b][j] = 0.f;
-
-  auto stage = [&](int t) {
-    char* l = lds + (t & 1) * BUF + tid * 16;
-    gload16(Asrc + (size_t)t * 32, (bf16_t*)l);
-    gload16(Asrc + (size_t)t * 32 + r64K, (bf16_t*)(l + 4096));
-    gload16(Bsrc + (size_t)t * 32, (bf16_t*)(l + 8192));
-    gload16(Bsrc + (size_t)t * 32 + r64K, (bf16_t*)(l + 12288));
-  };
-  auto rdA = [&](int buf, int row) -> bf16x8 {
-    int off = buf + (row << 6) + ((hi ^ ((row >> 1) & 3)) << 4);
-    return *(const bf16x8*)(lds + off);
-  };
-  auto rdB = [&](int buf, int row) -> bf16x8 {
-    int off = buf + 8192 + (row << 6) + ((hi ^ ((row >> 1) & 3)) << 4);
-    return *(const bf16x8*)(lds + off);
-  };
-
-  stage(0);
-
-  for (int t = 0; t < NT; ++t) {
-    VMCNT(0);
-    BARF();
-    const int buf = (t & 1) * BUF;
-    bf16x8 bfr[4], afr[4];
-#pragma unroll
-    for (int ni = 0; ni < 4; ++ni) bfr[ni] = rdB(buf, wn + ni * 16 + lr);
-#pragma unroll
-    for (int i = 0; i < 4; ++i) afr[i] = rdA(buf, wm + i * 16 + lr);
-    if (t + 1 < NT) stage(t + 1);
-    __builtin_amdgcn_s_setprio(1);
-#pragma unroll
-    for (int i = 0; i < 4; ++i)
-#pragma unroll
-      for (int ni = 0; ni < 4; ++ni)
-        acc[i][ni] = __builtin_amdgcn_mfma_f32_16x16x32_bf16(afr[i], bfr[ni], acc[i][ni], 0, 0, 0);
-    __builtin_amdgcn_s_setprio(0);
-  }
-
-  const float* bp = bias + (size_t)e * bstride;
-  float bv[4];
-#pragma unroll
-  for (int ni = 0; ni < 4; ++ni) bv[ni] = bp[bn + wn + ni * 16 + lr];
-#pragma unroll
-  for (int mi = 0; mi < 4; ++mi) {
-#pragma unroll
-    for (int j = 0; j < 4; ++j) {
-      const int slot = bm + wm + mi * 16 + hi * 4 + j;
-#pragma unroll
-      for (int ni = 0; ni < 4; ++ni) {
-        const int colg = bn + wn + ni * 16 + lr;
-        Cb[(size_t)slot * N + colg] = (bf16_t)(acc[mi][ni][j] + bv[ni]);
-      }
-    }
   }
 }
 
@@ -780,7 +823,6 @@
   int*    top2e = (int*)alloc((size_t)NTOK * 2 * 4);
   float*  top2w = (float*)alloc((size_t)NTOK * 2 * 4);
   int*    slotm = (int*)alloc((size_t)NTOK * 2 * 4);
-  int*    cnt   = (int*)alloc(NEXP * 4);
   int*    fill  = (int*)alloc(NEXP * 4);
   int*    basep = (int*)alloc((NEXP + 1) * 4);
   int*    ntl   = (int*)alloc(4);
@@ -788,38 +830,21 @@
   int*    t_row = (int*)alloc(MAXTILES * 4);
   int*    idx   = (int*)alloc(MAXROWS * 4);
   bf16_t* zpad  = (bf16_t*)alloc(256);
-  bf16_t* eo    = Dd;
-
-  k_f32_to_bf16<<<4096, 256, 0, stream>>>(x, xb, NTOK * DDIM / 8);
-  k_f32_to_bf16<<<4096, 256, 0, stream>>>(d1W, wd1, 2 * HDIM * DDIM / 8);
-  k_f32_to_bf16<<<2048, 256, 0, stream>>>(d2W, wd2, DDIM * HDIM / 8);
-  k_f32_to_bf16<<<512, 256, 0, stream>>>(sWin, wsin, SDIM * DDIM / 8);
-  k_convw<<<2048, 256, 0, stream>>>(sWc, wconv);
-  k_f32_to_bf16<<<512, 256, 0, stream>>>(sWo, wsout, DDIM * SDIM / 8);
-  k_f32_to_bf16<<<4096, 256, 0, stream>>>(eW1, we1, NEXP * 2 * HEXP * DDIM / 8);
-  k_f32_to_bf16<<<2048, 256, 0, stream>>>(eW2, we2, NEXP * DDIM * HEXP / 8);
-  k_zero<<<(MAXROWS + 255) / 256, 256, 0, stream>>>(cnt, fill, idx, zpad);
-  k_router<<<2048, 256, 0, stream>>>(x, rW, rb, mW, mb, bw3, top2e, top2w);
-  k_count<<<1, 1024, 0, stream>>>(top2e, cnt);
-  k_scan<<<1, 64, 0, stream>>>(cnt, basep, ntl, t_e, t_row);
+  bf16_t* eo = Dd;
+  bf16_t* mo = Dd + (size_t)18 * 1024 * 1024;
+
+  k_setup<<<21572, 256, 0, stream>>>(
+      x, d1W, d2W, sWin, sWo, eW1, eW2, sWc, rW, rb, mW, mb,
+      xb, wd1, wd2, wsin, wsout, we1, we2, wconv,
+      bw3, top2e, top2w, fill, idx, zpad);
+  k_count_scan<<<1, 1024, 0, stream>>>(top2e, basep, ntl, t_e, t_row);
   k_scatter<<<NTOK / 256, 256, 0, stream>>>(top2e, top2w, basep, fill, idx, slotm);
 
-  k_gemm_fc1<<<dim3(64, 64), 256, 0, stream>>>(
-      xb, wd1, wd1 + (size_t)HDIM * DDIM, Cc, d1b, d1b + HDIM, HDIM, DDIM);
-  k_gemm<EPI_OUT_W><<<dim3(8, 64), 256, 0, stream>>>(
-      Cc, wd2, nullptr, out, d2b, bw3, 3, DDIM, HDIM);
-
-  k_moe_fc1<<<dim3(MAXTILES, 8), 256, 0, stream>>>(
-      xb, we1, (size_t)2 * HEXP * DDIM, Cc, eb1, 2 * HEXP,
-      ntl, t_e, t_row, idx, HEXP, DDIM);
-  k_moe_fc2<<<dim3(MAXTILES, 8), 256, 0, stream>>>(
-      Cc, we2, (size_t)DDIM * HEXP, eo, eb2, DDIM,
-      ntl, t_e, t_row, DDIM, HEXP);
+  k_phase1<<<5696, 256, 0, stream>>>(
+      xb, wd1, d1b, Cc, we1, eb1, mo, ntl, t_e, t_row, idx, wsin, sbin, th);
+  k_phase2<<<2112, 256, 0, stream>>>(
+      Cc, wd2, d2b, bw3, out, th, wconv, sbc, tsq, zpad,
+      mo, we2, eb2, eo, ntl, t_e, t_row);
+  k_wsout<<<512, 256, 0, stream>>>(tsq, wsout, out, sbo, bw3);
   k_combine<<<NTOK / 4, 256, 0, stream>>>(eo, slotm, top2w, out);
-
-  k_gemm<EPI_BF16><<<dim3(8, 64), 256, 0, stream>>>(
-      xb, wsin, th, nullptr, sbin, nullptr, 0, SDIM, DDIM);
-  k_gemm_conv<<<dim3(8, 64), 256, 0, stream>>>(th, wconv, tsq, sbc, zpad);
-  k_gemm<EPI_OUT_A><<<dim3(8, 64), 256, 0, stream>>>(
-      tsq, wsout, nullptr, out, sbo, bw3 + 1, 3, DDIM, SDIM);
-}
+}
```

After: 589.0 us (median of 3 runs). No clear change (-0.9%).
